# Optimization experiments

Hardware: AMD Instinct MI355X
Metric: run time of the kernel (lower is better)

Reference implementation:

```python
import jax, jax.numpy as jnp
from jax import lax
import numpy as np

V, D, H, E, L, B = 512, 128, 64, 4, 60, 4096
ADJ = 184  # ((180 + 7) // 8) * 8


def setup_inputs() -> dict:
    key = jax.random.key(0)
    it = iter(jax.random.split(key, 64))

    def nrm(shape, s=0.05):
        return jax.random.normal(next(it), shape, dtype=jnp.float32) * s

    x = jax.random.randint(next(it), (B, L), 0, V, dtype=jnp.int32)
    inp = {"x": x, "emb": nrm((V, D), 0.02).at[0].set(0.0)}  # padding_idx=0 row zero
    for d in ("f", "r"):
        inp[f"w_ih_{d}"] = nrm((4 * H, D)); inp[f"w_hh_{d}"] = nrm((4 * H, H))
        inp[f"b_ih_{d}"] = nrm((4 * H,)); inp[f"b_hh_{d}"] = nrm((4 * H,))
    for p, i_, h_, o_ in (("e", 1, 16, 8), ("l", 1, 16, 8), ("c", V, 32, 16), ("p", 6, 24, 12), ("x", 4, 16, 8)):
        inp[f"{p}_w1"] = nrm((h_, i_)); inp[f"{p}_b1"] = nrm((h_,))
        inp[f"{p}_w2"] = nrm((o_, h_)); inp[f"{p}_b2"] = nrm((o_,))
    inp["fp_w"] = nrm((ADJ, 180)); inp["fp_b"] = nrm((ADJ,))
    inp["attn_w"] = nrm((3 * ADJ, ADJ)); inp["attn_b"] = nrm((3 * ADJ,))
    inp["out_w"] = nrm((ADJ, ADJ)); inp["out_b"] = nrm((ADJ,))
    for i, (o_, i_) in enumerate(((128, ADJ), (64, 128), (32, 64), (E, 32)), 1):
        inp[f"g_w{i}"] = nrm((o_, i_)); inp[f"g_b{i}"] = nrm((o_,))
    return inp


def _mlp2(h, w1, b1, w2, b2):
    return jnp.maximum(h @ w1.T + b1, 0.0) @ w2.T + b2


def _lstm_final(xe, w_ih, w_hh, b_ih, b_hh):
    # torch LSTM gate order i, f, g, o; returns final hidden state [B, H]
    xg = jnp.einsum('bld,gd->blg', xe, w_ih) + b_ih
    h0 = jnp.zeros((xe.shape[0], H), xe.dtype)

    def step(carry, g_t):
        h, c = carry
        g = g_t + h @ w_hh.T + b_hh
        i, f, gg, o = jnp.split(g, 4, axis=-1)
        c = jax.nn.sigmoid(f) * c + jax.nn.sigmoid(i) * jnp.tanh(gg)
        h = jax.nn.sigmoid(o) * jnp.tanh(c)
        return (h, c), None

    (h, _), _ = lax.scan(step, (h0, h0), jnp.swapaxes(xg, 0, 1))
    return h


def _sequence_stats(x):
    # Fully vectorized equivalent of the per-sequence python loops
    f32 = jnp.float32
    mask = x != 0
    vlen = mask.sum(1)                                       # [B]
    vlenf = jnp.maximum(vlen, 1).astype(f32)
    pos = jnp.arange(L)
    # per-row histogram over valid tokens (torch.bincount of valid_seq)
    counts = jnp.zeros((B, V), f32).at[jnp.arange(B)[:, None], x].add(mask.astype(f32))
    probs = counts / jnp.maximum(counts.sum(1, keepdims=True), 1.0)
    entropy = -jnp.sum(probs * jnp.log(probs + 1e-8), axis=1)
    entropy = jnp.where(vlen > 1, entropy, 0.0)
    char_dist = counts / vlenf[:, None]
    # compact valid tokens to the front (torch: seq[seq != 0]), stable argsort
    order = jnp.argsort((~mask).astype(jnp.int32), axis=1)
    cseq = jnp.take_along_axis(x, order, axis=1)
    cseq = jnp.where(pos[None] < vlen[:, None], cseq, 0)
    a, b = cseq[:, :-1], cseq[:, 1:]
    pairmask = pos[: L - 1][None] < (vlen - 1)[:, None]
    den1 = jnp.maximum(vlen - 1, 1).astype(f32)
    repeat = ((a == b) & pairmask).sum(1) / den1
    inc = ((b > a) & pairmask).sum(1) / den1
    dec = ((b < a) & pairmask).sum(1) / den1
    m2 = pos[: L - 2][None] < (vlen - 2)[:, None]
    per = ((cseq[:, :-2] == cseq[:, 2:]) & m2).sum(1) / jnp.maximum(vlen - 2, 1)
    per = jnp.where(vlen >= 4, per, 0.0)
    diversity = (counts > 0).sum(1) / vlenf
    # longest run of equal consecutive tokens via cummax of reset positions
    eq = jnp.concatenate([jnp.zeros((B, 1), bool), (cseq[:, 1:] == cseq[:, :-1]) & (pos[1:][None] < vlen[:, None])], 1)
    lastreset = lax.cummax(jnp.where(eq, -1, pos[None]), axis=1)
    runlen = pos[None] - lastreset + 1
    max_rep = jnp.where(pos[None] < vlen[:, None], runlen, 0).max(1) / vlenf
    pattern = jnp.stack([repeat, inc, dec, per, diversity, max_rep], 1).astype(f32)
    pattern = jnp.where((vlen > 1)[:, None], pattern, 0.0)
    # unique bigrams: sort pair codes, count distinct valid codes
    codes = jnp.where(pairmask, a * V + b, -1)
    s = jnp.sort(codes, axis=1)
    prevc = jnp.concatenate([jnp.full((B, 1), -2, s.dtype), s[:, :-1]], 1)
    comp_ratio = ((s != prevc) & (s >= 0)).sum(1) / den1
    info_density = entropy / jnp.log(jnp.maximum(vlen, 2).astype(f32))
    # local complexity: mean over sliding windows of (#unique / w), w = min(5, len//2)
    wsel = jnp.minimum(5, vlen // 2)
    local = jnp.zeros((B,), f32)
    for w in (2, 3, 4, 5):
        nwin = L - w + 1
        sh = [cseq[:, k:k + nwin] for k in range(w)]
        u = jnp.ones((B, nwin), f32)
        for k in range(1, w):
            isnew = jnp.ones((B, nwin), bool)
            for m in range(k):
                isnew = isnew & (sh[k] != sh[m])
            u = u + isnew
        winmask = pos[:nwin][None] < (vlen - w + 1)[:, None]
        lc = (u * winmask).sum(1) / w / jnp.maximum(vlen - w + 1, 1)
        local = jnp.where(wsel == w, lc, local)
    trans = 1.0 - repeat  # transitions/(len-1) == 1 - repeat_ratio
    complexity = jnp.stack([comp_ratio, info_density, local, trans], 1).astype(f32)
    complexity = jnp.where((vlen > 1)[:, None], complexity, 0.0)
    return entropy, vlen, char_dist, pattern, complexity


def reference(x, emb, w_ih_f, w_hh_f, b_ih_f, b_hh_f, w_ih_r, w_hh_r, b_ih_r, b_hh_r, e_w1, e_b1, e_w2, e_b2, l_w1, l_b1, l_w2, l_b2, c_w1, c_b1, c_w2, c_b2, p_w1, p_b1, p_w2, p_b2, x_w1, x_b1, x_w2, x_b2, fp_w, fp_b, attn_w, attn_b, out_w, out_b, g_w1, g_b1, g_w2, g_b2, g_w3, g_b3, g_w4, g_b4):
    entropy, vlen, char_dist, pattern, complexity = _sequence_stats(x)
    xe = emb[x]                                               # [B, L, D]
    h_f = _lstm_final(xe, w_ih_f, w_hh_f, b_ih_f, b_hh_f)
    h_r = _lstm_final(xe[:, ::-1], w_ih_r, w_hh_r, b_ih_r, b_hh_r)
    feats = jnp.concatenate([
        h_f, h_r,
        _mlp2((entropy / 4.0)[:, None], e_w1, e_b1, e_w2, e_b2),
        _mlp2((vlen.astype(jnp.float32) / 60.0)[:, None], l_w1, l_b1, l_w2, l_b2),
        _mlp2(char_dist, c_w1, c_b1, c_w2, c_b2),
        _mlp2(pattern, p_w1, p_b1, p_w2, p_b2),
        _mlp2(complexity, x_w1, x_b1, x_w2, x_b2),
    ], axis=1)                                                # [B, 180]
    f = feats @ fp_w.T + fp_b                                 # [B, 184]
    # MultiheadAttention with seq_len == 1: softmax over a single key is 1,
    # so attended = out_proj(v_proj(f)) exactly (q/k projections cancel).
    wv, bv = attn_w[2 * ADJ:], attn_b[2 * ADJ:]
    attended = (f @ wv.T + bv) @ out_w.T + out_b
    h = jnp.maximum(attended @ g_w1.T + g_b1, 0.0)
    h = jnp.maximum(h @ g_w2.T + g_b2, 0.0)
    h = jnp.maximum(h @ g_w3.T + g_b3, 0.0)
    logits = h @ g_w4.T + g_b4
    return jax.nn.softmax(logits, axis=-1)  # eval path (training=False)
```

## Files before the change

### kernel.cpp

```cpp
#include <hip/hip_runtime.h>

#define BATCH 4096
#define SEQL  60
#define VOC   512
#define EMBD  128
#define HID   64
#define GATES 256
#define ADJ   184

typedef __attribute__((ext_vector_type(8))) short short8;
typedef __attribute__((ext_vector_type(4))) float f32x4;

__device__ __forceinline__ float sigm(float x) {
  return __builtin_amdgcn_rcpf(1.f + __expf(-x));
}
__device__ __forceinline__ float tanh_(float x) {
  float e = __expf(2.f * x);
  return 1.f - 2.f * __builtin_amdgcn_rcpf(e + 1.f);
}
__device__ __forceinline__ unsigned short f2bf_rne(float f) {
  unsigned int u = __float_as_uint(f);
  unsigned int r = (u + 0x7fffu + ((u >> 16) & 1u)) >> 16;
  return (unsigned short)r;
}
__device__ __forceinline__ unsigned short f2bf(float f) {
  return (unsigned short)((__float_as_uint(f) + 0x8000u) >> 16);
}
__device__ __forceinline__ float dot4(float4 a, float4 b, float acc) {
  acc = fmaf(a.x, b.x, acc); acc = fmaf(a.y, b.y, acc);
  acc = fmaf(a.z, b.z, acc); acc = fmaf(a.w, b.w, acc);
  return acc;
}
__device__ __forceinline__ float wsumf(float v) {
  #pragma unroll
  for (int s = 32; s > 0; s >>= 1) v += __shfl_xor(v, s, 64);
  return v;
}
__device__ __forceinline__ int wsumi(int v) {
  #pragma unroll
  for (int s = 32; s > 0; s >>= 1) v += __shfl_xor(v, s, 64);
  return v;
}
__device__ __forceinline__ int wmaxi(int v) {
  #pragma unroll
  for (int s = 32; s > 0; s >>= 1) v = max(v, __shfl_xor(v, s, 64));
  return v;
}

__global__ __launch_bounds__(256) void k_prep(
    const float* __restrict__ emb,
    const float* __restrict__ wih_f, const float* __restrict__ bif, const float* __restrict__ bhf,
    const float* __restrict__ wih_r, const float* __restrict__ bir, const float* __restrict__ bhr,
    const float* __restrict__ whh_f, const float* __restrict__ whh_r,
    const float* __restrict__ g_w1, const float* __restrict__ g_b1,
    const float* __restrict__ out_w, const float* __restrict__ out_b,
    const float* __restrict__ attn_w, const float* __restrict__ attn_b,
    const float* __restrict__ fp_w, const float* __restrict__ fp_b,
    const float* __restrict__ g_w2, const float* __restrict__ g_w3,
    const float* __restrict__ g_w4, const float* __restrict__ c_w1,
    float* __restrict__ G_f, float* __restrict__ G_r,
    unsigned short* __restrict__ Wfrag,
    float* __restrict__ A, float* __restrict__ avb,
    float* __restrict__ Bp, float* __restrict__ vb,
    float* __restrict__ g_w2t, float* __restrict__ g_w3t, float* __restrict__ g_w4t,
    float* __restrict__ c_w1t) {
  const int bid = blockIdx.x;
  const int tid = threadIdx.x;

  if (bid < 128) {
    const int dir = bid >> 6;
    const int rem = bid & 63;
    const int v0 = (rem >> 2) * 32;
    const int j0 = (rem & 3) * 64;
    const float* W = dir ? wih_r : wih_f;
    const float* bi = dir ? bir : bif;
    const float* bh = dir ? bhr : bhf;
    float* G = dir ? G_r : G_f;
    const int vp = tid >> 4;
    const int jq = tid & 15;
    const int v = v0 + vp * 2;
    const int j = j0 + jq * 4;
    const int gg = j >> 6;
    const int u0 = j & 63;

    const float4* E0 = (const float4*)(emb + (size_t)v * 128);
    const float4* E1 = (const float4*)(emb + (size_t)(v + 1) * 128);
    const float4* W0 = (const float4*)(W + (size_t)j * 128);
    const float4* W1 = (const float4*)(W + (size_t)(j + 1) * 128);
    const float4* W2 = (const float4*)(W + (size_t)(j + 2) * 128);
    const float4* W3 = (const float4*)(W + (size_t)(j + 3) * 128);

    float a00 = 0.f, a01 = 0.f, a02 = 0.f, a03 = 0.f;
    float a10 = 0.f, a11 = 0.f, a12 = 0.f, a13 = 0.f;
    #pragma unroll 4
    for (int d4 = 0; d4 < 32; d4++) {
      float4 e0 = E0[d4], e1 = E1[d4];
      float4 w0 = W0[d4], w1 = W1[d4], w2 = W2[d4], w3 = W3[d4];
      a00 = dot4(e0, w0, a00); a01 = dot4(e0, w1, a01);
      a02 = dot4(e0, w2, a02); a03 = dot4(e0, w3, a03);
      a10 = dot4(e1, w0, a10); a11 = dot4(e1, w1, a11);
      a12 = dot4(e1, w2, a12); a13 = dot4(e1, w3, a13);
    }
    float b0v = bi[j] + bh[j], b1v = bi[j + 1] + bh[j + 1];
    float b2v = bi[j + 2] + bh[j + 2], b3v = bi[j + 3] + bh[j + 3];
    float* g0 = G + (size_t)v * 256 + u0 * 4 + gg;
    g0[0]  = a00 + b0v; g0[4]  = a01 + b1v;
    g0[8]  = a02 + b2v; g0[12] = a03 + b3v;
    float* g1 = g0 + 256;
    g1[0]  = a10 + b0v; g1[4]  = a11 + b1v;
    g1[8]  = a12 + b2v; g1[12] = a13 + b3v;
  } else if (bid < 144) {
    const int id = (bid - 128) * 256 + tid;
    const int lane = id & 63;
    const int fc = id >> 6;
    const int c = fc & 1;
    const int gg = (fc >> 1) & 3;
    const int w = (fc >> 3) & 3;
    const int dir = fc >> 5;
    const float* whh = dir ? whh_r : whh_f;
    const int n = gg * 64 + w * 16 + (lane & 15);
    const int kb = c * 32 + (lane >> 4) * 8;
    unsigned short* o = Wfrag + (size_t)id * 8;
    #pragma unroll
    for (int j = 0; j < 8; j++) o[j] = f2bf_rne(whh[n * 64 + kb + j]);
  } else if (bid < 272) {
    const int i = bid - 144;
    const int j = tid;
    const float* g1r = g_w1 + (size_t)i * ADJ;
    if (j < ADJ) {
      float a0 = 0.f, a1 = 0.f, a2 = 0.f, a3 = 0.f;
      for (int k = 0; k < ADJ; k += 4) {
        a0 = fmaf(g1r[k],     out_w[(size_t)(k)     * ADJ + j], a0);
        a1 = fmaf(g1r[k + 1], out_w[(size_t)(k + 1) * ADJ + j], a1);
        a2 = fmaf(g1r[k + 2], out_w[(size_t)(k + 2) * ADJ + j], a2);
        a3 = fmaf(g1r[k + 3], out_w[(size_t)(k + 3) * ADJ + j], a3);
      }
      A[(size_t)i * ADJ + j] = (a0 + a1) + (a2 + a3);
    } else if (j == ADJ) {
      float a0 = 0.f;
      for (int k = 0; k < ADJ; k++) a0 = fmaf(g1r[k], out_b[k], a0);
      avb[i] = a0 + g_b1[i];
    }
  } else if (bid < 456) {
    const int k = bid - 272;
    const int j = tid;
    const float* wvr = attn_w + (size_t)(2 * ADJ + k) * ADJ;
    if (j < 180) {
      float a0 = 0.f, a1 = 0.f, a2 = 0.f, a3 = 0.f;
      for (int m = 0; m < ADJ; m += 4) {
        a0 = fmaf(wvr[m],     fp_w[(size_t)(m)     * 180 + j], a0);
        a1 = fmaf(wvr[m + 1], fp_w[(size_t)(m + 1) * 180 + j], a1);
        a2 = fmaf(wvr[m + 2], fp_w[(size_t)(m + 2) * 180 + j], a2);
        a3 = fmaf(wvr[m + 3], fp_w[(size_t)(m + 3) * 180 + j], a3);
      }
      Bp[(size_t)k * 180 + j] = (a0 + a1) + (a2 + a3);
    } else if (j == 180) {
      float a0 = 0.f;
      for (int m = 0; m < ADJ; m++) a0 = fmaf(wvr[m], fp_b[m], a0);
      vb[k] = a0 + attn_b[2 * ADJ + k];
    }
  } else if (bid == 456) {
    for (int i = tid; i < 64 * 128; i += 256) {
      int o = i >> 7, k = i & 127;
      g_w2t[k * 64 + o] = g_w2[i];
    }
    for (int i = tid; i < 32 * 64; i += 256) {
      int o = i >> 6, k = i & 63;
      g_w3t[k * 32 + o] = g_w3[i];
    }
    if (tid < 128) {
      int o = tid >> 5, k = tid & 31;
      g_w4t[k * 4 + o] = g_w4[tid];
    }
  } else {
    const int base = (bid - 457) * 2048;
    for (int i = tid; i < 2048; i += 256) {
      int idx = base + i;
      int o = idx >> 9, k = idx & 511;
      c_w1t[k * 32 + o] = k ? c_w1[o * 512 + k] : 0.f;
    }
  }
}

#define LSTM_STEP(T, CUR, NXT)                                                 \
  {                                                                            \
    const unsigned short* hb = hbuf[(T) & 1];                                  \
    short8 a0 = *(const short8*)(hb + ln * 72 + kg * 8);                       \
    short8 a1 = *(const short8*)(hb + ln * 72 + 32 + kg * 8);                  \
    if ((T) < 59) {                                                            \
      int tsn = dir ? (58 - (T)) : ((T) + 1);                                  \
      uint4 of4 = *(const uint4*)(tokoff + tsn * 16 + kg * 4);                 \
      NXT[0] = *(const float4*)(Gb + of4.x + ub);                              \
      NXT[1] = *(const float4*)(Gb + of4.y + ub);                              \
      NXT[2] = *(const float4*)(Gb + of4.z + ub);                              \
      NXT[3] = *(const float4*)(Gb + of4.w + ub);                              \
    }                                                                          \
    f32x4 z0 = {0.f, 0.f, 0.f, 0.f};                                           \
    f32x4 acc0 = z0, acc1 = z0, acc2 = z0, acc3 = z0;                          \
    acc0 = __builtin_amdgcn_mfma_f32_16x16x32_bf16(a0, bfr[0][0], acc0, 0, 0, 0); \
    acc1 = __builtin_amdgcn_mfma_f32_16x16x32_bf16(a0, bfr[1][0], acc1, 0, 0, 0); \
    acc2 = __builtin_amdgcn_mfma_f32_16x16x32_bf16(a0, bfr[2][0], acc2, 0, 0, 0); \
    acc3 = __builtin_amdgcn_mfma_f32_16x16x32_bf16(a0, bfr[3][0], acc3, 0, 0, 0); \
    acc0 = __builtin_amdgcn_mfma_f32_16x16x32_bf16(a1, bfr[0][1], acc0, 0, 0, 0); \
    acc1 = __builtin_amdgcn_mfma_f32_16x16x32_bf16(a1, bfr[1][1], acc1, 0, 0, 0); \
    acc2 = __builtin_amdgcn_mfma_f32_16x16x32_bf16(a1, bfr[2][1], acc2, 0, 0, 0); \
    acc3 = __builtin_amdgcn_mfma_f32_16x16x32_bf16(a1, bfr[3][1], acc3, 0, 0, 0); \
    unsigned short* hw = hbuf[((T) + 1) & 1];                                  \
    _Pragma("unroll")                                                          \
    for (int r = 0; r < 4; r++) {                                              \
      float gi = acc0[r] + CUR[r].x;                                           \
      float gf = acc1[r] + CUR[r].y;                                           \
      float gc = acc2[r] + CUR[r].z;                                           \
      float go = acc3[r] + CUR[r].w;                                           \
      float cn = sigm(gf) * cst[r] + sigm(gi) * tanh_(gc);                     \
      cst[r] = cn;                                                             \
      float h = sigm(go) * tanh_(cn);                                          \
      hw[(kg * 4 + r) * 72 + u] = f2bf(h);                                     \
      if ((T) == 59) ho[(size_t)(b0 + kg * 4 + r) * 64 + u] = h;               \
    }                                                                          \
    __syncthreads();                                                           \
  }

__global__ __launch_bounds__(256) void k_main(
    const int* __restrict__ x,
    const float* __restrict__ G_f, const float* __restrict__ G_r,
    const unsigned short* __restrict__ Wfrag,
    const float* __restrict__ A, const float* __restrict__ avb,
    const float* __restrict__ Bp, const float* __restrict__ vb,
    float* __restrict__ C1t, float* __restrict__ c1b,
    float* __restrict__ hf_o, float* __restrict__ hr_o,
    float* __restrict__ ent_o, float* __restrict__ vlen_o,
    float* __restrict__ pat_o, float* __restrict__ cpx_o) {
  __shared__ __align__(16) unsigned short hbuf[2][16 * 72];
  __shared__ __align__(16) unsigned int tokoff[60 * 16];
  __shared__ unsigned int cnt[4][512];
  __shared__ unsigned short q[4][68];
  const int bid = blockIdx.x;
  const int tid = threadIdx.x;

  if (bid < 512) {
    const int lane = tid & 63;
    const int w = tid >> 6;
    const int dir = bid >> 8;
    const int blk = bid & 255;
    const int b0 = blk << 4;
    const float* G = dir ? G_r : G_f;
    const char* Gb = (const char*)G;
    float* ho = dir ? hr_o : hf_o;

    for (int i = tid; i < 960; i += 256) {
      int r = i / 60, t = i - r * 60;
      tokoff[t * 16 + r] = ((unsigned int)x[(size_t)(b0 + r) * 60 + t]) << 10;
    }
    for (int i = tid; i < 16 * 72; i += 256) hbuf[0][i] = 0;

    short8 bfr[4][2];
    #pragma unroll
    for (int gg = 0; gg < 4; gg++)
      #pragma unroll
      for (int c = 0; c < 2; c++) {
        int idx = (((dir * 4 + w) * 4 + gg) * 2 + c) * 64 + lane;
        bfr[gg][c] = *(const short8*)(Wfrag + (size_t)idx * 8);
      }

    const int kg = lane >> 4;
    const int ln = lane & 15;
    const int u = w * 16 + ln;
    const unsigned int ub = (unsigned int)u * 16;
    float cst[4] = {0.f, 0.f, 0.f, 0.f};
    float4 gvA[4], gvB[4];

    __syncthreads();

    {
      int ts0 = dir ? 59 : 0;
      uint4 of4 = *(const uint4*)(tokoff + ts0 * 16 + kg * 4);
      gvA[0] = *(const float4*)(Gb + of4.x + ub);
      gvA[1] = *(const float4*)(Gb + of4.y + ub);
      gvA[2] = *(const float4*)(Gb + of4.z + ub);
      gvA[3] = *(const float4*)(Gb + of4.w + ub);
    }

    #pragma unroll 1
    for (int tt = 0; tt < 30; tt++) {
      const int t0 = tt * 2, t1 = tt * 2 + 1;
      LSTM_STEP(t0, gvA, gvB)
      LSTM_STEP(t1, gvB, gvA)
    }
  } else if (bid < 1536) {
    const int lane = tid & 63;
    const int wid = tid >> 6;
    const int row = (bid - 512) * 4 + wid;
    unsigned int* cr = cnt[wid];
    unsigned short* qr = q[wid];

    for (int i = lane; i < 512; i += 64) cr[i] = 0u;
    qr[lane] = 0;
    if (lane < 4) qr[64 + lane] = 0;
    int v = (lane < 60) ? x[row * 60 + lane] : 0;
    bool act = (v != 0);
    unsigned long long amask = __ballot(act);
    int n = __popcll(amask);
    __syncthreads();
    if (act) {
      int pos = __popcll(amask & ((1ull << lane) - 1ull));
      qr[pos] = (unsigned short)v;
      atomicAdd(&cr[v], 1u);
    }
    __syncthreads();

    float vlenf = (float)(n >= 1 ? n : 1);
    float inv = 1.f / vlenf;

    float ent = 0.f; int distinct = 0;
    #pragma unroll
    for (int j = 0; j < 8; j++) {
      unsigned int c = cr[lane + j * 64];
      if (c) {
        distinct++;
        float p = (float)c * inv;
        ent -= p * __logf(p + 1e-8f);
      }
    }
    ent = wsumf(ent);
    distinct = wsumi(distinct);

    int a = qr[lane], b = qr[lane + 1], c2 = qr[lane + 2];
    bool v1 = (lane + 1 < n);
    bool v2 = (lane + 2 < n);
    int rep  = __popcll(__ballot(v1 && (a == b)));
    int incs = __popcll(__ballot(v1 && (b > a)));
    int decs = __popcll(__ballot(v1 && (b < a)));
    int per2 = __popcll(__ballot(v2 && (a == c2)));

    int prev = (lane > 0) ? (int)qr[lane - 1] : -1;
    bool isst = (lane < n) && (lane == 0 || a != prev);
    unsigned long long smask = __ballot(isst);
    int len = 0;
    if (isst) {
      unsigned long long hi = (lane < 63) ? (smask >> (lane + 1)) : 0ull;
      int next = hi ? (lane + __ffsll((unsigned long long)hi)) : n;
      len = next - lane;
    }
    int maxrun = wmaxi(len);

    int code = v1 ? (a * VOC + b) : -1;
    int unique = v1 ? 1 : 0;
    #pragma unroll 1
    for (int j = 0; j < 58; j++) {
      int cj = __shfl(code, j, 64);
      if (j < lane && cj == code) unique = 0;
    }
    int dc = __popcll(__ballot(unique != 0));

    int wl = n >> 1; if (wl > 5) wl = 5;
    float local = 0.f;
    if (wl >= 2) {
      bool pv = (lane + wl <= n);
      int u = 0;
      if (pv) {
        int t0 = qr[lane], t1 = qr[lane + 1], t2 = qr[lane + 2];
        int t3 = qr[lane + 3], t4 = qr[lane + 4];
        u = 1;
        u += (t1 != t0);
        if (wl >= 3) u += (int)((t2 != t1) && (t2 != t0));
        if (wl >= 4) u += (int)((t3 != t2) && (t3 != t1) && (t3 != t0));
        if (wl >= 5) u += (int)((t4 != t3) && (t4 != t2) && (t4 != t1) && (t4 != t0));
      }
      int usum = wsumi(u);
      int denw = n - wl + 1; if (denw < 1) denw = 1;
      local = (float)usum / (float)wl / (float)denw;
    }

    float den1 = (float)((n - 1) >= 1 ? (n - 1) : 1);
    float repeat = (float)rep / den1;
    float per = (n >= 4) ? (float)per2 / (float)((n - 2) >= 1 ? (n - 2) : 1) : 0.f;
    float entz = (n > 1) ? ent : 0.f;
    float z = (n > 1) ? 1.f : 0.f;

    if (lane == 0) {
      ent_o[row] = entz;
      vlen_o[row] = (float)n;
      pat_o[row * 6 + 0] = repeat * z;
      pat_o[row * 6 + 1] = (float)incs / den1 * z;
      pat_o[row * 6 + 2] = (float)decs / den1 * z;
      pat_o[row * 6 + 3] = per * z;
      pat_o[row * 6 + 4] = (float)distinct * inv * z;
      pat_o[row * 6 + 5] = (float)maxrun * inv * z;
      cpx_o[row * 4 + 0] = (float)dc / den1 * z;
      cpx_o[row * 4 + 1] = entz / __logf((float)(n >= 2 ? n : 2)) * z;
      cpx_o[row * 4 + 2] = local * z;
      cpx_o[row * 4 + 3] = (1.f - repeat) * z;
    }
  } else {
    const int i = bid - 1536, j = tid;
    const float* Ar = A + (size_t)i * ADJ;
    if (j < 180) {
      float a0 = 0.f, a1 = 0.f, a2 = 0.f, a3 = 0.f;
      for (int k = 0; k < ADJ; k += 4) {
        a0 = fmaf(Ar[k],     Bp[(size_t)(k)     * 180 + j], a0);
        a1 = fmaf(Ar[k + 1], Bp[(size_t)(k + 1) * 180 + j], a1);
        a2 = fmaf(Ar[k + 2], Bp[(size_t)(k + 2) * 180 + j], a2);
        a3 = fmaf(Ar[k + 3], Bp[(size_t)(k + 3) * 180 + j], a3);
      }
      C1t[(size_t)j * 128 + i] = (a0 + a1) + (a2 + a3);
    } else if (j == 180) {
      float a0 = 0.f;
      for (int k = 0; k < ADJ; k++) a0 = fmaf(Ar[k], vb[k], a0);
      c1b[i] = a0 + avb[i];
    }
  }
}

#define FSTR 192

__global__ __launch_bounds__(256) void k_head(
    const int* __restrict__ x,
    const float* __restrict__ hf, const float* __restrict__ hr,
    const float* __restrict__ ent, const float* __restrict__ vlen,
    const float* __restrict__ pat, const float* __restrict__ cpx,
    const float* __restrict__ e_w1, const float* __restrict__ e_b1,
    const float* __restrict__ e_w2, const float* __restrict__ e_b2,
    const float* __restrict__ l_w1, const float* __restrict__ l_b1,
    const float* __restrict__ l_w2, const float* __restrict__ l_b2,
    const float* __restrict__ c_w1t, const float* __restrict__ c_b1,
    const float* __restrict__ c_w2, const float* __restrict__ c_b2,
    const float* __restrict__ p_w1, const float* __restrict__ p_b1,
    const float* __restrict__ p_w2, const float* __restrict__ p_b2,
    const float* __restrict__ x_w1, const float* __restrict__ x_b1,
    const float* __restrict__ x_w2, const float* __restrict__ x_b2,
    const float* __restrict__ C1t, const float* __restrict__ c1b,
    const float* __restrict__ g_w2t, const float* __restrict__ g_b2,
    const float* __restrict__ g_w3t, const float* __restrict__ g_b3,
    const float* __restrict__ g_w4t, const float* __restrict__ g_b4,
    float* __restrict__ out) {
  __shared__ float feat[8 * FSTR];
  __shared__ unsigned short tk[8 * 64];
  __shared__ float h1[8 * 128];
  __shared__ float h2[8 * 64];
  __shared__ float h3[8 * 32];
  __shared__ float h1c[8 * 33];
  __shared__ float lg[32];
  const int tid = threadIdx.x;
  const int b0 = blockIdx.x * 8;

  if (tid < 128) {
    int r = tid >> 4, c = tid & 15;
    float4 vv = ((const float4*)(hf + (size_t)(b0 + r) * 64))[c];
    *(float4*)(feat + r * FSTR + c * 4) = vv;
  } else {
    int t = tid - 128;
    int r = t >> 4, c = t & 15;
    float4 vv = ((const float4*)(hr + (size_t)(b0 + r) * 64))[c];
    *(float4*)(feat + r * FSTR + 64 + c * 4) = vv;
  }
  for (int i = tid; i < 480; i += 256) {
    int r = i / 60, t = i - r * 60;
    tk[r * 64 + t] = (unsigned short)x[(size_t)(b0 + r) * 60 + t];
  }
  __syncthreads();
  {
    int o = tid & 31, r = tid >> 5;
    const unsigned short* tkr = tk + r * 64;
    float a0 = 0.f, a1 = 0.f, a2 = 0.f, a3 = 0.f;
    #pragma unroll 5
    for (int t = 0; t < 60; t += 4) {
      int t0 = tkr[t], t1 = tkr[t + 1], t2 = tkr[t + 2], t3 = tkr[t + 3];
      a0 += c_w1t[t0 * 32 + o];
      a1 += c_w1t[t1 * 32 + o];
      a2 += c_w1t[t2 * 32 + o];
      a3 += c_w1t[t3 * 32 + o];
    }
    float invv = __builtin_amdgcn_rcpf(fmaxf(vlen[b0 + r], 1.f));
    h1c[r * 33 + o] = fmaxf(((a0 + a1) + (a2 + a3)) * invv + c_b1[o], 0.f);
  }
  __syncthreads();
  if (tid < 32) {
    const int m = tid & 3, r = tid >> 2, b = b0 + r;
    float tt[24];
    if (m == 0) {
      float ein = ent[b] * 0.25f;
      #pragma unroll
      for (int o = 0; o < 16; o++) tt[o] = fmaxf(e_w1[o] * ein + e_b1[o], 0.f);
      #pragma unroll
      for (int o = 0; o < 8; o++) {
        float a = e_b2[o];
        #pragma unroll
        for (int k = 0; k < 16; k++) a = fmaf(e_w2[o * 16 + k], tt[k], a);
        feat[r * FSTR + 128 + o] = a;
      }
    } else if (m == 1) {
      float lin = vlen[b] * (1.f / 60.f);
      #pragma unroll
      for (int o = 0; o < 16; o++) tt[o] = fmaxf(l_w1[o] * lin + l_b1[o], 0.f);
      #pragma unroll
      for (int o = 0; o < 8; o++) {
        float a = l_b2[o];
        #pragma unroll
        for (int k = 0; k < 16; k++) a = fmaf(l_w2[o * 16 + k], tt[k], a);
        feat[r * FSTR + 136 + o] = a;
      }
    } else if (m == 2) {
      float pin[6];
      #pragma unroll
      for (int k = 0; k < 6; k++) pin[k] = pat[b * 6 + k];
      #pragma unroll
      for (int o = 0; o < 24; o++) {
        float a = p_b1[o];
        #pragma unroll
        for (int k = 0; k < 6; k++) a = fmaf(p_w1[o * 6 + k], pin[k], a);
        tt[o] = fmaxf(a, 0.f);
      }
      #pragma unroll
      for (int o = 0; o < 12; o++) {
        float a = p_b2[o];
        #pragma unroll
        for (int k = 0; k < 24; k++) a = fmaf(p_w2[o * 24 + k], tt[k], a);
        feat[r * FSTR + 160 + o] = a;
      }
    } else {
      float xin[4];
      #pragma unroll
      for (int k = 0; k < 4; k++) xin[k] = cpx[b * 4 + k];
      #pragma unroll
      for (int o = 0; o < 16; o++) {
        float a = x_b1[o];
        #pragma unroll
        for (int k = 0; k < 4; k++) a = fmaf(x_w1[o * 4 + k], xin[k], a);
        tt[o] = fmaxf(a, 0.f);
      }
      #pragma unroll
      for (int o = 0; o < 8; o++) {
        float a = x_b2[o];
        #pragma unroll
        for (int k = 0; k < 16; k++) a = fmaf(x_w2[o * 16 + k], tt[k], a);
        feat[r * FSTR + 172 + o] = a;
      }
    }
  } else if (tid >= 64 && tid < 192) {
    int t = tid - 64;
    int r = t >> 4, o = t & 15;
    float a = c_b2[o];
    const float* hh = h1c + r * 33;
    #pragma unroll
    for (int k = 0; k < 32; k++) a = fmaf(c_w2[o * 32 + k], hh[k], a);
    feat[r * FSTR + 144 + o] = a;
  }
  __syncthreads();

  {
    const int o = tid & 127, rg = tid >> 7;
    const float* f0p = feat + (rg * 4 + 0) * FSTR;
    const float* f1p = feat + (rg * 4 + 1) * FSTR;
    const float* f2p = feat + (rg * 4 + 2) * FSTR;
    const float* f3p = feat + (rg * 4 + 3) * FSTR;
    float a0 = 0.f, a1 = 0.f, a2 = 0.f, a3 = 0.f;
    #pragma unroll 3
    for (int k4 = 0; k4 < 45; k4++) {
      float w0 = C1t[(size_t)(k4 * 4 + 0) * 128 + o];
      float w1 = C1t[(size_t)(k4 * 4 + 1) * 128 + o];
      float w2 = C1t[(size_t)(k4 * 4 + 2) * 128 + o];
      float w3 = C1t[(size_t)(k4 * 4 + 3) * 128 + o];
      float4 f0 = *(const float4*)(f0p + k4 * 4);
      float4 f1 = *(const float4*)(f1p + k4 * 4);
      float4 f2 = *(const float4*)(f2p + k4 * 4);
      float4 f3 = *(const float4*)(f3p + k4 * 4);
      a0 = fmaf(w0, f0.x, a0); a0 = fmaf(w1, f0.y, a0);
      a0 = fmaf(w2, f0.z, a0); a0 = fmaf(w3, f0.w, a0);
      a1 = fmaf(w0, f1.x, a1); a1 = fmaf(w1, f1.y, a1);
      a1 = fmaf(w2, f1.z, a1); a1 = fmaf(w3, f1.w, a1);
      a2 = fmaf(w0, f2.x, a2); a2 = fmaf(w1, f2.y, a2);
      a2 = fmaf(w2, f2.z, a2); a2 = fmaf(w3, f2.w, a2);
      a3 = fmaf(w0, f3.x, a3); a3 = fmaf(w1, f3.y, a3);
      a3 = fmaf(w2, f3.z, a3); a3 = fmaf(w3, f3.w, a3);
    }
    float bb = c1b[o];
    h1[(rg * 4 + 0) * 128 + o] = fmaxf(a0 + bb, 0.f);
    h1[(rg * 4 + 1) * 128 + o] = fmaxf(a1 + bb, 0.f);
    h1[(rg * 4 + 2) * 128 + o] = fmaxf(a2 + bb, 0.f);
    h1[(rg * 4 + 3) * 128 + o] = fmaxf(a3 + bb, 0.f);
  }
  __syncthreads();
  {
    const int o = tid & 63, rg = tid >> 6;
    const float* f0p = h1 + (rg * 2 + 0) * 128;
    const float* f1p = h1 + (rg * 2 + 1) * 128;
    float a0 = 0.f, a1 = 0.f;
    #pragma unroll 4
    for (int k4 = 0; k4 < 32; k4++) {
      float w0 = g_w2t[(k4 * 4 + 0) * 64 + o];
      float w1 = g_w2t[(k4 * 4 + 1) * 64 + o];
      float w2 = g_w2t[(k4 * 4 + 2) * 64 + o];
      float w3 = g_w2t[(k4 * 4 + 3) * 64 + o];
      float4 f0 = *(const float4*)(f0p + k4 * 4);
      float4 f1 = *(const float4*)(f1p + k4 * 4);
      a0 = fmaf(w0, f0.x, a0); a0 = fmaf(w1, f0.y, a0);
      a0 = fmaf(w2, f0.z, a0); a0 = fmaf(w3, f0.w, a0);
      a1 = fmaf(w0, f1.x, a1); a1 = fmaf(w1, f1.y, a1);
      a1 = fmaf(w2, f1.z, a1); a1 = fmaf(w3, f1.w, a1);
    }
    float bb = g_b2[o];
    h2[(rg * 2 + 0) * 64 + o] = fmaxf(a0 + bb, 0.f);
    h2[(rg * 2 + 1) * 64 + o] = fmaxf(a1 + bb, 0.f);
  }
  __syncthreads();
  {
    const int o = tid & 31, rg = tid >> 5;
    const float* fp = h2 + rg * 64;
    float a = 0.f;
    #pragma unroll 4
    for (int k4 = 0; k4 < 16; k4++) {
      float w0 = g_w3t[(k4 * 4 + 0) * 32 + o];
      float w1 = g_w3t[(k4 * 4 + 1) * 32 + o];
      float w2 = g_w3t[(k4 * 4 + 2) * 32 + o];
      float w3 = g_w3t[(k4 * 4 + 3) * 32 + o];
      float4 f0 = *(const float4*)(fp + k4 * 4);
      a = fmaf(w0, f0.x, a); a = fmaf(w1, f0.y, a);
      a = fmaf(w2, f0.z, a); a = fmaf(w3, f0.w, a);
    }
    h3[rg * 32 + o] = fmaxf(a + g_b3[o], 0.f);
  }
  __syncthreads();
  if (tid < 32) {
    int r = tid >> 2, o = tid & 3;
    const float* hh = h3 + r * 32;
    float a = g_b4[o];
    #pragma unroll
    for (int k = 0; k < 32; k++) a = fmaf(g_w4t[k * 4 + o], hh[k], a);
    lg[tid] = a;
  }
  __syncthreads();
  if (tid < 8) {
    float l0 = lg[tid * 4 + 0], l1 = lg[tid * 4 + 1];
    float l2 = lg[tid * 4 + 2], l3 = lg[tid * 4 + 3];
    float m = fmaxf(fmaxf(l0, l1), fmaxf(l2, l3));
    float e0 = __expf(l0 - m), e1 = __expf(l1 - m);
    float e2 = __expf(l2 - m), e3 = __expf(l3 - m);
    float is = __builtin_amdgcn_rcpf(e0 + e1 + e2 + e3);
    float4 o4; o4.x = e0 * is; o4.y = e1 * is; o4.z = e2 * is; o4.w = e3 * is;
    *(float4*)(out + (size_t)(b0 + tid) * 4) = o4;
  }
}

extern "C" void kernel_launch(void* const* d_in, const int* in_sizes, int n_in,
                              void* d_out, int out_size, void* d_ws, size_t ws_size,
                              hipStream_t stream) {
  const int*   x     = (const int*)d_in[0];
  const float* emb   = (const float*)d_in[1];
  const float* wih_f = (const float*)d_in[2];
  const float* whh_f = (const float*)d_in[3];
  const float* bih_f = (const float*)d_in[4];
  const float* bhh_f = (const float*)d_in[5];
  const float* wih_r = (const float*)d_in[6];
  const float* whh_r = (const float*)d_in[7];
  const float* bih_r = (const float*)d_in[8];
  const float* bhh_r = (const float*)d_in[9];
  const float* e_w1 = (const float*)d_in[10]; const float* e_b1 = (const float*)d_in[11];
  const float* e_w2 = (const float*)d_in[12]; const float* e_b2 = (const float*)d_in[13];
  const float* l_w1 = (const float*)d_in[14]; const float* l_b1 = (const float*)d_in[15];
  const float* l_w2 = (const float*)d_in[16]; const float* l_b2 = (const float*)d_in[17];
  const float* c_w1 = (const float*)d_in[18]; const float* c_b1 = (const float*)d_in[19];
  const float* c_w2 = (const float*)d_in[20]; const float* c_b2 = (const float*)d_in[21];
  const float* p_w1 = (const float*)d_in[22]; const float* p_b1 = (const float*)d_in[23];
  const float* p_w2 = (const float*)d_in[24]; const float* p_b2 = (const float*)d_in[25];
  const float* x_w1 = (const float*)d_in[26]; const float* x_b1 = (const float*)d_in[27];
  const float* x_w2 = (const float*)d_in[28]; const float* x_b2 = (const float*)d_in[29];
  const float* fp_w = (const float*)d_in[30]; const float* fp_b = (const float*)d_in[31];
  const float* attn_w = (const float*)d_in[32]; const float* attn_b = (const float*)d_in[33];
  const float* out_w = (const float*)d_in[34]; const float* out_b = (const float*)d_in[35];
  const float* g_w1 = (const float*)d_in[36]; const float* g_b1 = (const float*)d_in[37];
  const float* g_w2 = (const float*)d_in[38]; const float* g_b2 = (const float*)d_in[39];
  const float* g_w3 = (const float*)d_in[40]; const float* g_b3 = (const float*)d_in[41];
  const float* g_w4 = (const float*)d_in[42]; const float* g_b4 = (const float*)d_in[43];

  float* ws   = (float*)d_ws;
  float* G_f  = ws;
  float* G_r  = G_f  + 512 * 256;
  float* hfw  = G_r  + 512 * 256;
  float* hrw  = hfw  + BATCH * 64;
  float* entw = hrw  + BATCH * 64;
  float* vlnw = entw + BATCH;
  float* patw = vlnw + BATCH;
  float* cpxw = patw + BATCH * 6;
  float* Aw   = cpxw + BATCH * 4;
  float* avbw = Aw + 128 * ADJ;
  float* Bpw  = avbw + 128;
  float* vbw  = Bpw + ADJ * 180;
  float* C1t  = vbw + ADJ;
  float* c1b  = C1t + 180 * 128;
  float* g2t  = c1b + 128;
  float* g3t  = g2t + 128 * 64;
  float* g4t  = g3t + 64 * 32;
  float* cw1t = g4t + 32 * 4;
  unsigned short* Wfrag = (unsigned short*)(cw1t + 512 * 32);

  k_prep<<<dim3(465), dim3(256), 0, stream>>>(
      emb, wih_f, bih_f, bhh_f, wih_r, bih_r, bhh_r, whh_f, whh_r,
      g_w1, g_b1, out_w, out_b, attn_w, attn_b, fp_w, fp_b,
      g_w2, g_w3, g_w4, c_w1,
      G_f, G_r, Wfrag, Aw, avbw, Bpw, vbw, g2t, g3t, g4t, cw1t);
  k_main<<<dim3(1664), dim3(256), 0, stream>>>(
      x, G_f, G_r, Wfrag, Aw, avbw, Bpw, vbw, C1t, c1b,
      hfw, hrw, entw, vlnw, patw, cpxw);
  k_head<<<dim3(BATCH / 8), dim3(256), 0, stream>>>(
      x, hfw, hrw, entw, vlnw, patw, cpxw,
      e_w1, e_b1, e_w2, e_b2, l_w1, l_b1, l_w2, l_b2,
      cw1t, c_b1, c_w2, c_b2, p_w1, p_b1, p_w2, p_b2,
      x_w1, x_b1, x_w2, x_b2, C1t, c1b,
      g2t, g_b2, g3t, g_b3, g4t, g_b4,
      (float*)d_out);
}
```

Measured before the change: 247.3 us.

## Fuse head kernel into main kernel using global flag-based dependencies

Merges the separate head kernel into the main kernel as extra blocks. The head blocks wait on per-block global flags set by the LSTM, stats and prep2 blocks, with a counter for the C1 matrix build. Shared memory becomes a single overlaid byte buffer, and arguments move into one struct. The intent is to remove a launch boundary and let head work overlap the tail of the LSTM. This relies on spin-waiting blocks making forward progress, which risks deadlock or stalls if waiting blocks occupy slots needed by the producer blocks. It also adds a memset launch.

```diff
diff --git a/kernel.cpp b/kernel.cpp
--- a/kernel.cpp
+++ b/kernel.cpp
@@ -3,9 +3,6 @@
 #define BATCH 4096
 #define SEQL  60
 #define VOC   512
-#define EMBD  128
-#define HID   64
-#define GATES 256
 #define ADJ   184
 
 typedef __attribute__((ext_vector_type(8))) short short8;
@@ -20,8 +17,7 @@
 }
 __device__ __forceinline__ unsigned short f2bf_rne(float f) {
   unsigned int u = __float_as_uint(f);
-  unsigned int r = (u + 0x7fffu + ((u >> 16) & 1u)) >> 16;
-  return (unsigned short)r;
+  return (unsigned short)((u + 0x7fffu + ((u >> 16) & 1u)) >> 16);
 }
 __device__ __forceinline__ unsigned short f2bf(float f) {
   return (unsigned short)((__float_as_uint(f) + 0x8000u) >> 16);
@@ -47,23 +43,37 @@
   return v;
 }
 
-__global__ __launch_bounds__(256) void k_prep(
-    const float* __restrict__ emb,
-    const float* __restrict__ wih_f, const float* __restrict__ bif, const float* __restrict__ bhf,
-    const float* __restrict__ wih_r, const float* __restrict__ bir, const float* __restrict__ bhr,
-    const float* __restrict__ whh_f, const float* __restrict__ whh_r,
-    const float* __restrict__ g_w1, const float* __restrict__ g_b1,
-    const float* __restrict__ out_w, const float* __restrict__ out_b,
-    const float* __restrict__ attn_w, const float* __restrict__ attn_b,
-    const float* __restrict__ fp_w, const float* __restrict__ fp_b,
-    const float* __restrict__ g_w2, const float* __restrict__ g_w3,
-    const float* __restrict__ g_w4, const float* __restrict__ c_w1,
-    float* __restrict__ G_f, float* __restrict__ G_r,
-    unsigned short* __restrict__ Wfrag,
-    float* __restrict__ A, float* __restrict__ avb,
-    float* __restrict__ Bp, float* __restrict__ vb,
-    float* __restrict__ g_w2t, float* __restrict__ g_w3t, float* __restrict__ g_w4t,
-    float* __restrict__ c_w1t) {
+struct KP {
+  const int* x;
+  const float *emb, *wih_f, *bif, *bhf, *wih_r, *bir, *bhr, *whh_f, *whh_r;
+  const float *e_w1, *e_b1, *e_w2, *e_b2, *l_w1, *l_b1, *l_w2, *l_b2;
+  const float *c_w1, *c_b1, *c_w2, *c_b2, *p_w1, *p_b1, *p_w2, *p_b2;
+  const float *x_w1, *x_b1, *x_w2, *x_b2;
+  const float *fp_w, *fp_b, *attn_w, *attn_b, *out_w, *out_b;
+  const float *g_w1, *g_b1, *g_w2, *g_b2, *g_w3, *g_b3, *g_w4, *g_b4;
+  float *G_f, *G_r;
+  unsigned short* Wfrag;
+  float *A, *avb, *Bp, *vb, *C1t, *c1b, *g2t, *g3t, *g4t, *cw1t;
+  float *hf, *hr, *ent, *vlen, *pat, *cpx;
+  int *lflag, *sflag, *p2ctr;
+  float* out;
+};
+
+#define SM_BYTES 15616
+#define SM_HBUF  0
+#define SM_TOK   4608
+#define SM_CNT   0
+#define SM_Q     8192
+#define SM_FEAT  0
+#define SM_TK    6144
+#define SM_H1    7168
+#define SM_H2    11264
+#define SM_H3    13312
+#define SM_H1C   14336
+#define SM_LG    15392
+#define FSTR 192
+
+__global__ __launch_bounds__(256) void k_prep(KP p) {
   const int bid = blockIdx.x;
   const int tid = threadIdx.x;
 
@@ -72,19 +82,17 @@
     const int rem = bid & 63;
     const int v0 = (rem >> 2) * 32;
     const int j0 = (rem & 3) * 64;
-    const float* W = dir ? wih_r : wih_f;
-    const float* bi = dir ? bir : bif;
-    const float* bh = dir ? bhr : bhf;
-    float* G = dir ? G_r : G_f;
-    const int vp = tid >> 4;
-    const int jq = tid & 15;
-    const int v = v0 + vp * 2;
-    const int j = j0 + jq * 4;
+    const float* W = dir ? p.wih_r : p.wih_f;
+    const float* bi = dir ? p.bir : p.bif;
+    const float* bh = dir ? p.bhr : p.bhf;
+    float* G = dir ? p.G_r : p.G_f;
+    const int v = v0 + (tid >> 4) * 2;
+    const int j = j0 + (tid & 15) * 4;
     const int gg = j >> 6;
     const int u0 = j & 63;
 
-    const float4* E0 = (const float4*)(emb + (size_t)v * 128);
-    const float4* E1 = (const float4*)(emb + (size_t)(v + 1) * 128);
+    const float4* E0 = (const float4*)(p.emb + (size_t)v * 128);
+    const float4* E1 = (const float4*)(p.emb + (size_t)(v + 1) * 128);
     const float4* W0 = (const float4*)(W + (size_t)j * 128);
     const float4* W1 = (const float4*)(W + (size_t)(j + 1) * 128);
     const float4* W2 = (const float4*)(W + (size_t)(j + 2) * 128);
@@ -117,74 +125,74 @@
     const int gg = (fc >> 1) & 3;
     const int w = (fc >> 3) & 3;
     const int dir = fc >> 5;
-    const float* whh = dir ? whh_r : whh_f;
+    const float* whh = dir ? p.whh_r : p.whh_f;
     const int n = gg * 64 + w * 16 + (lane & 15);
     const int kb = c * 32 + (lane >> 4) * 8;
-    unsigned short* o = Wfrag + (size_t)id * 8;
+    unsigned short* o = p.Wfrag + (size_t)id * 8;
     #pragma unroll
     for (int j = 0; j < 8; j++) o[j] = f2bf_rne(whh[n * 64 + kb + j]);
   } else if (bid < 272) {
     const int i = bid - 144;
     const int j = tid;
-    const float* g1r = g_w1 + (size_t)i * ADJ;
+    const float* g1r = p.g_w1 + (size_t)i * ADJ;
     if (j < ADJ) {
       float a0 = 0.f, a1 = 0.f, a2 = 0.f, a3 = 0.f;
       for (int k = 0; k < ADJ; k += 4) {
-        a0 = fmaf(g1r[k],     out_w[(size_t)(k)     * ADJ + j], a0);
-        a1 = fmaf(g1r[k + 1], out_w[(size_t)(k + 1) * ADJ + j], a1);
-        a2 = fmaf(g1r[k + 2], out_w[(size_t)(k + 2) * ADJ + j], a2);
-        a3 = fmaf(g1r[k + 3], out_w[(size_t)(k + 3) * ADJ + j], a3);
+        a0 = fmaf(g1r[k],     p.out_w[(size_t)(k)     * ADJ + j], a0);
+        a1 = fmaf(g1r[k + 1], p.out_w[(size_t)(k + 1) * ADJ + j], a1);
+        a2 = fmaf(g1r[k + 2], p.out_w[(size_t)(k + 2) * ADJ + j], a2);
+        a3 = fmaf(g1r[k + 3], p.out_w[(size_t)(k + 3) * ADJ + j], a3);
       }
-      A[(size_t)i * ADJ + j] = (a0 + a1) + (a2 + a3);
+      p.A[(size_t)i * ADJ + j] = (a0 + a1) + (a2 + a3);
     } else if (j == ADJ) {
       float a0 = 0.f;
-      for (int k = 0; k < ADJ; k++) a0 = fmaf(g1r[k], out_b[k], a0);
-      avb[i] = a0 + g_b1[i];
+      for (int k = 0; k < ADJ; k++) a0 = fmaf(g1r[k], p.out_b[k], a0);
+      p.avb[i] = a0 + p.g_b1[i];
     }
   } else if (bid < 456) {
     const int k = bid - 272;
     const int j = tid;
-    const float* wvr = attn_w + (size_t)(2 * ADJ + k) * ADJ;
+    const float* wvr = p.attn_w + (size_t)(2 * ADJ + k) * ADJ;
     if (j < 180) {
       float a0 = 0.f, a1 = 0.f, a2 = 0.f, a3 = 0.f;
       for (int m = 0; m < ADJ; m += 4) {
-        a0 = fmaf(wvr[m],     fp_w[(size_t)(m)     * 180 + j], a0);
-        a1 = fmaf(wvr[m + 1], fp_w[(size_t)(m + 1) * 180 + j], a1);
-        a2 = fmaf(wvr[m + 2], fp_w[(size_t)(m + 2) * 180 + j], a2);
-        a3 = fmaf(wvr[m + 3], fp_w[(size_t)(m + 3) * 180 + j], a3);
+        a0 = fmaf(wvr[m],     p.fp_w[(size_t)(m)     * 180 + j], a0);
+        a1 = fmaf(wvr[m + 1], p.fp_w[(size_t)(m + 1) * 180 + j], a1);
+        a2 = fmaf(wvr[m + 2], p.fp_w[(size_t)(m + 2) * 180 + j], a2);
+        a3 = fmaf(wvr[m + 3], p.fp_w[(size_t)(m + 3) * 180 + j], a3);
       }
-      Bp[(size_t)k * 180 + j] = (a0 + a1) + (a2 + a3);
+      p.Bp[(size_t)k * 180 + j] = (a0 + a1) + (a2 + a3);
     } else if (j == 180) {
       float a0 = 0.f;
-      for (int m = 0; m < ADJ; m++) a0 = fmaf(wvr[m], fp_b[m], a0);
-      vb[k] = a0 + attn_b[2 * ADJ + k];
+      for (int m = 0; m < ADJ; m++) a0 = fmaf(wvr[m], p.fp_b[m], a0);
+      p.vb[k] = a0 + p.attn_b[2 * ADJ + k];
     }
   } else if (bid == 456) {
     for (int i = tid; i < 64 * 128; i += 256) {
       int o = i >> 7, k = i & 127;
-      g_w2t[k * 64 + o] = g_w2[i];
+      p.g2t[k * 64 + o] = p.g_w2[i];
     }
     for (int i = tid; i < 32 * 64; i += 256) {
       int o = i >> 6, k = i & 63;
-      g_w3t[k * 32 + o] = g_w3[i];
+      p.g3t[k * 32 + o] = p.g_w3[i];
     }
     if (tid < 128) {
       int o = tid >> 5, k = tid & 31;
-      g_w4t[k * 4 + o] = g_w4[tid];
+      p.g4t[k * 4 + o] = p.g_w4[tid];
     }
   } else {
     const int base = (bid - 457) * 2048;
     for (int i = tid; i < 2048; i += 256) {
       int idx = base + i;
       int o = idx >> 9, k = idx & 511;
-      c_w1t[k * 32 + o] = k ? c_w1[o * 512 + k] : 0.f;
+      p.cw1t[k * 32 + o] = k ? p.c_w1[o * 512 + k] : 0.f;
     }
   }
 }
 
 #define LSTM_STEP(T, CUR, NXT)                                                 \
   {                                                                            \
-    const unsigned short* hb = hbuf[(T) & 1];                                  \
+    const unsigned short* hb = hbuf + ((T) & 1) * (16 * 72);                   \
     short8 a0 = *(const short8*)(hb + ln * 72 + kg * 8);                       \
     short8 a1 = *(const short8*)(hb + ln * 72 + 32 + kg * 8);                  \
     if ((T) < 59) {                                                            \
@@ -205,7 +213,7 @@
     acc1 = __builtin_amdgcn_mfma_f32_16x16x32_bf16(a1, bfr[1][1], acc1, 0, 0, 0); \
     acc2 = __builtin_amdgcn_mfma_f32_16x16x32_bf16(a1, bfr[2][1], acc2, 0, 0, 0); \
     acc3 = __builtin_amdgcn_mfma_f32_16x16x32_bf16(a1, bfr[3][1], acc3, 0, 0, 0); \
-    unsigned short* hw = hbuf[((T) + 1) & 1];                                  \
+    unsigned short* hw = hbuf + (((T) + 1) & 1) * (16 * 72);                   \
     _Pragma("unroll")                                                          \
     for (int r = 0; r < 4; r++) {                                              \
       float gi = acc0[r] + CUR[r].x;                                           \
@@ -221,242 +229,228 @@
     __syncthreads();                                                           \
   }
 
-__global__ __launch_bounds__(256) void k_main(
-    const int* __restrict__ x,
-    const float* __restrict__ G_f, const float* __restrict__ G_r,
-    const unsigned short* __restrict__ Wfrag,
-    const float* __restrict__ A, const float* __restrict__ avb,
-    const float* __restrict__ Bp, const float* __restrict__ vb,
-    float* __restrict__ C1t, float* __restrict__ c1b,
-    float* __restrict__ hf_o, float* __restrict__ hr_o,
-    float* __restrict__ ent_o, float* __restrict__ vlen_o,
-    float* __restrict__ pat_o, float* __restrict__ cpx_o) {
-  __shared__ __align__(16) unsigned short hbuf[2][16 * 72];
-  __shared__ __align__(16) unsigned int tokoff[60 * 16];
-  __shared__ unsigned int cnt[4][512];
-  __shared__ unsigned short q[4][68];
-  const int bid = blockIdx.x;
-  const int tid = threadIdx.x;
-
-  if (bid < 512) {
-    const int lane = tid & 63;
-    const int w = tid >> 6;
-    const int dir = bid >> 8;
-    const int blk = bid & 255;
-    const int b0 = blk << 4;
-    const float* G = dir ? G_r : G_f;
-    const char* Gb = (const char*)G;
-    float* ho = dir ? hr_o : hf_o;
-
-    for (int i = tid; i < 960; i += 256) {
-      int r = i / 60, t = i - r * 60;
-      tokoff[t * 16 + r] = ((unsigned int)x[(size_t)(b0 + r) * 60 + t]) << 10;
-    }
-    for (int i = tid; i < 16 * 72; i += 256) hbuf[0][i] = 0;
-
-    short8 bfr[4][2];
+__device__ void lstm_block(int bid, int tid, const KP& p, char* smem) {
+  unsigned short* hbuf = (unsigned short*)(smem + SM_HBUF);
+  unsigned int* tokoff = (unsigned int*)(smem + SM_TOK);
+  const int lane = tid & 63;
+  const int w = tid >> 6;
+  const int dir = bid >> 8;
+  const int blk = bid & 255;
+  const int b0 = blk << 4;
+  const float* G = dir ? p.G_r : p.G_f;
+  const char* Gb = (const char*)G;
+  float* ho = dir ? p.hr : p.hf;
+
+  for (int i = tid; i < 960; i += 256) {
+    int r = i / 60, t = i - r * 60;
+    tokoff[t * 16 + r] = ((unsigned int)p.x[(size_t)(b0 + r) * 60 + t]) << 10;
+  }
+  for (int i = tid; i < 16 * 72; i += 256) hbuf[i] = 0;
+
+  short8 bfr[4][2];
+  #pragma unroll
+  for (int gg = 0; gg < 4; gg++)
     #pragma unroll
-    for (int gg = 0; gg < 4; gg++)
-      #pragma unroll
-      for (int c = 0; c < 2; c++) {
-        int idx = (((dir * 4 + w) * 4 + gg) * 2 + c) * 64 + lane;
-        bfr[gg][c] = *(const short8*)(Wfrag + (size_t)idx * 8);
-      }
-
-    const int kg = lane >> 4;
-    const int ln = lane & 15;
-    const int u = w * 16 + ln;
-    const unsigned int ub = (unsigned int)u * 16;
-    float cst[4] = {0.f, 0.f, 0.f, 0.f};
-    float4 gvA[4], gvB[4];
-
-    __syncthreads();
-
-    {
-      int ts0 = dir ? 59 : 0;
-      uint4 of4 = *(const uint4*)(tokoff + ts0 * 16 + kg * 4);
-      gvA[0] = *(const float4*)(Gb + of4.x + ub);
-      gvA[1] = *(const float4*)(Gb + of4.y + ub);
-      gvA[2] = *(const float4*)(Gb + of4.z + ub);
-      gvA[3] = *(const float4*)(Gb + of4.w + ub);
-    }
-
-    #pragma unroll 1
-    for (int tt = 0; tt < 30; tt++) {
-      const int t0 = tt * 2, t1 = tt * 2 + 1;
-      LSTM_STEP(t0, gvA, gvB)
-      LSTM_STEP(t1, gvB, gvA)
-    }
-  } else if (bid < 1536) {
-    const int lane = tid & 63;
-    const int wid = tid >> 6;
-    const int row = (bid - 512) * 4 + wid;
-    unsigned int* cr = cnt[wid];
-    unsigned short* qr = q[wid];
-
-    for (int i = lane; i < 512; i += 64) cr[i] = 0u;
-    qr[lane] = 0;
-    if (lane < 4) qr[64 + lane] = 0;
-    int v = (lane < 60) ? x[row * 60 + lane] : 0;
-    bool act = (v != 0);
-    unsigned long long amask = __ballot(act);
-    int n = __popcll(amask);
-    __syncthreads();
-    if (act) {
-      int pos = __popcll(amask & ((1ull << lane) - 1ull));
-      qr[pos] = (unsigned short)v;
-      atomicAdd(&cr[v], 1u);
-    }
-    __syncthreads();
-
-    float vlenf = (float)(n >= 1 ? n : 1);
-    float inv = 1.f / vlenf;
-
-    float ent = 0.f; int distinct = 0;
-    #pragma unroll
-    for (int j = 0; j < 8; j++) {
-      unsigned int c = cr[lane + j * 64];
-      if (c) {
-        distinct++;
-        float p = (float)c * inv;
-        ent -= p * __logf(p + 1e-8f);
-      }
-    }
-    ent = wsumf(ent);
-    distinct = wsumi(distinct);
-
-    int a = qr[lane], b = qr[lane + 1], c2 = qr[lane + 2];
-    bool v1 = (lane + 1 < n);
-    bool v2 = (lane + 2 < n);
-    int rep  = __popcll(__ballot(v1 && (a == b)));
-    int incs = __popcll(__ballot(v1 && (b > a)));
-    int decs = __popcll(__ballot(v1 && (b < a)));
-    int per2 = __popcll(__ballot(v2 && (a == c2)));
-
-    int prev = (lane > 0) ? (int)qr[lane - 1] : -1;
-    bool isst = (lane < n) && (lane == 0 || a != prev);
-    unsigned long long smask = __ballot(isst);
-    int len = 0;
-    if (isst) {
-      unsigned long long hi = (lane < 63) ? (smask >> (lane + 1)) : 0ull;
-      int next = hi ? (lane + __ffsll((unsigned long long)hi)) : n;
-      len = next - lane;
-    }
-    int maxrun = wmaxi(len);
-
-    int code = v1 ? (a * VOC + b) : -1;
-    int unique = v1 ? 1 : 0;
-    #pragma unroll 1
-    for (int j = 0; j < 58; j++) {
-      int cj = __shfl(code, j, 64);
-      if (j < lane && cj == code) unique = 0;
-    }
-    int dc = __popcll(__ballot(unique != 0));
-
-    int wl = n >> 1; if (wl > 5) wl = 5;
-    float local = 0.f;
-    if (wl >= 2) {
-      bool pv = (lane + wl <= n);
-      int u = 0;
-      if (pv) {
-        int t0 = qr[lane], t1 = qr[lane + 1], t2 = qr[lane + 2];
-        int t3 = qr[lane + 3], t4 = qr[lane + 4];
-        u = 1;
-        u += (t1 != t0);
-        if (wl >= 3) u += (int)((t2 != t1) && (t2 != t0));
-        if (wl >= 4) u += (int)((t3 != t2) && (t3 != t1) && (t3 != t0));
-        if (wl >= 5) u += (int)((t4 != t3) && (t4 != t2) && (t4 != t1) && (t4 != t0));
-      }
-      int usum = wsumi(u);
-      int denw = n - wl + 1; if (denw < 1) denw = 1;
-      local = (float)usum / (float)wl / (float)denw;
-    }
-
-    float den1 = (float)((n - 1) >= 1 ? (n - 1) : 1);
-    float repeat = (float)rep / den1;
-    float per = (n >= 4) ? (float)per2 / (float)((n - 2) >= 1 ? (n - 2) : 1) : 0.f;
-    float entz = (n > 1) ? ent : 0.f;
-    float z = (n > 1) ? 1.f : 0.f;
-
-    if (lane == 0) {
-      ent_o[row] = entz;
-      vlen_o[row] = (float)n;
-      pat_o[row * 6 + 0] = repeat * z;
-      pat_o[row * 6 + 1] = (float)incs / den1 * z;
-      pat_o[row * 6 + 2] = (float)decs / den1 * z;
-      pat_o[row * 6 + 3] = per * z;
-      pat_o[row * 6 + 4] = (float)distinct * inv * z;
-      pat_o[row * 6 + 5] = (float)maxrun * inv * z;
-      cpx_o[row * 4 + 0] = (float)dc / den1 * z;
-      cpx_o[row * 4 + 1] = entz / __logf((float)(n >= 2 ? n : 2)) * z;
-      cpx_o[row * 4 + 2] = local * z;
-      cpx_o[row * 4 + 3] = (1.f - repeat) * z;
-    }
-  } else {
-    const int i = bid - 1536, j = tid;
-    const float* Ar = A + (size_t)i * ADJ;
-    if (j < 180) {
-      float a0 = 0.f, a1 = 0.f, a2 = 0.f, a3 = 0.f;
-      for (int k = 0; k < ADJ; k += 4) {
-        a0 = fmaf(Ar[k],     Bp[(size_t)(k)     * 180 + j], a0);
-        a1 = fmaf(Ar[k + 1], Bp[(size_t)(k + 1) * 180 + j], a1);
-        a2 = fmaf(Ar[k + 2], Bp[(size_t)(k + 2) * 180 + j], a2);
-        a3 = fmaf(Ar[k + 3], Bp[(size_t)(k + 3) * 180 + j], a3);
-      }
-      C1t[(size_t)j * 128 + i] = (a0 + a1) + (a2 + a3);
-    } else if (j == 180) {
-      float a0 = 0.f;
-      for (int k = 0; k < ADJ; k++) a0 = fmaf(Ar[k], vb[k], a0);
-      c1b[i] = a0 + avb[i];
-    }
-  }
-}
-
-#define FSTR 192
-
-__global__ __launch_bounds__(256) void k_head(
-    const int* __restrict__ x,
-    const float* __restrict__ hf, const float* __restrict__ hr,
-    const float* __restrict__ ent, const float* __restrict__ vlen,
-    const float* __restrict__ pat, const float* __restrict__ cpx,
-    const float* __restrict__ e_w1, const float* __restrict__ e_b1,
-    const float* __restrict__ e_w2, const float* __restrict__ e_b2,
-    const float* __restrict__ l_w1, const float* __restrict__ l_b1,
-    const float* __restrict__ l_w2, const float* __restrict__ l_b2,
-    const float* __restrict__ c_w1t, const float* __restrict__ c_b1,
-    const float* __restrict__ c_w2, const float* __restrict__ c_b2,
-    const float* __restrict__ p_w1, const float* __restrict__ p_b1,
-    const float* __restrict__ p_w2, const float* __restrict__ p_b2,
-    const float* __restrict__ x_w1, const float* __restrict__ x_b1,
-    const float* __restrict__ x_w2, const float* __restrict__ x_b2,
-    const float* __restrict__ C1t, const float* __restrict__ c1b,
-    const float* __restrict__ g_w2t, const float* __restrict__ g_b2,
-    const float* __restrict__ g_w3t, const float* __restrict__ g_b3,
-    const float* __restrict__ g_w4t, const float* __restrict__ g_b4,
-    float* __restrict__ out) {
-  __shared__ float feat[8 * FSTR];
-  __shared__ unsigned short tk[8 * 64];
-  __shared__ float h1[8 * 128];
-  __shared__ float h2[8 * 64];
-  __shared__ float h3[8 * 32];
-  __shared__ float h1c[8 * 33];
-  __shared__ float lg[32];
-  const int tid = threadIdx.x;
-  const int b0 = blockIdx.x * 8;
+    for (int c = 0; c < 2; c++) {
+      int idx = (((dir * 4 + w) * 4 + gg) * 2 + c) * 64 + lane;
+      bfr[gg][c] = *(const short8*)(p.Wfrag + (size_t)idx * 8);
+    }
+
+  const int kg = lane >> 4;
+  const int ln = lane & 15;
+  const int u = w * 16 + ln;
+  const unsigned int ub = (unsigned int)u * 16;
+  float cst[4] = {0.f, 0.f, 0.f, 0.f};
+  float4 gvA[4], gvB[4];
+
+  __syncthreads();
+
+  {
+    int ts0 = dir ? 59 : 0;
+    uint4 of4 = *(const uint4*)(tokoff + ts0 * 16 + kg * 4);
+    gvA[0] = *(const float4*)(Gb + of4.x + ub);
+    gvA[1] = *(const float4*)(Gb + of4.y + ub);
+    gvA[2] = *(const float4*)(Gb + of4.z + ub);
+    gvA[3] = *(const float4*)(Gb + of4.w + ub);
+  }
+
+  #pragma unroll 1
+  for (int tt = 0; tt < 30; tt++) {
+    const int t0 = tt * 2, t1 = tt * 2 + 1;
+    LSTM_STEP(t0, gvA, gvB)
+    LSTM_STEP(t1, gvB, gvA)
+  }
+  __threadfence();
+  __syncthreads();
+  if (tid == 0) atomicExch(&p.lflag[bid], 1);
+}
+
+__device__ void prep2_block(int i, int j, const KP& p) {
+  const float* Ar = p.A + (size_t)i * ADJ;
+  if (j < 180) {
+    float a0 = 0.f, a1 = 0.f, a2 = 0.f, a3 = 0.f;
+    for (int k = 0; k < ADJ; k += 4) {
+      a0 = fmaf(Ar[k],     p.Bp[(size_t)(k)     * 180 + j], a0);
+      a1 = fmaf(Ar[k + 1], p.Bp[(size_t)(k + 1) * 180 + j], a1);
+      a2 = fmaf(Ar[k + 2], p.Bp[(size_t)(k + 2) * 180 + j], a2);
+      a3 = fmaf(Ar[k + 3], p.Bp[(size_t)(k + 3) * 180 + j], a3);
+    }
+    p.C1t[(size_t)j * 128 + i] = (a0 + a1) + (a2 + a3);
+  } else if (j == 180) {
+    float a0 = 0.f;
+    for (int k = 0; k < ADJ; k++) a0 = fmaf(Ar[k], p.vb[k], a0);
+    p.c1b[i] = a0 + p.avb[i];
+  }
+  __threadfence();
+  __syncthreads();
+  if (j == 0) atomicAdd(p.p2ctr, 1);
+}
+
+__device__ void stats_block(int s, int tid, const KP& p, char* smem) {
+  unsigned int* cntb = (unsigned int*)(smem + SM_CNT);
+  unsigned short* qb = (unsigned short*)(smem + SM_Q);
+  const int lane = tid & 63;
+  const int wid = tid >> 6;
+  const int row = s * 4 + wid;
+  unsigned int* cr = cntb + wid * 512;
+  unsigned short* qr = qb + wid * 68;
+
+  for (int i = lane; i < 512; i += 64) cr[i] = 0u;
+  qr[lane] = 0;
+  if (lane < 4) qr[64 + lane] = 0;
+  int v = (lane < 60) ? p.x[row * 60 + lane] : 0;
+  bool act = (v != 0);
+  unsigned long long amask = __ballot(act);
+  int n = __popcll(amask);
+  __syncthreads();
+  if (act) {
+    int pos = __popcll(amask & ((1ull << lane) - 1ull));
+    qr[pos] = (unsigned short)v;
+    atomicAdd(&cr[v], 1u);
+  }
+  __syncthreads();
+
+  float vlenf = (float)(n >= 1 ? n : 1);
+  float inv = 1.f / vlenf;
+
+  float ent = 0.f; int distinct = 0;
+  #pragma unroll
+  for (int j = 0; j < 8; j++) {
+    unsigned int c = cr[lane + j * 64];
+    if (c) {
+      distinct++;
+      float pr = (float)c * inv;
+      ent -= pr * __logf(pr + 1e-8f);
+    }
+  }
+  ent = wsumf(ent);
+  distinct = wsumi(distinct);
+
+  int a = qr[lane], b = qr[lane + 1], c2 = qr[lane + 2];
+  bool v1 = (lane + 1 < n);
+  bool v2 = (lane + 2 < n);
+  int rep  = __popcll(__ballot(v1 && (a == b)));
+  int incs = __popcll(__ballot(v1 && (b > a)));
+  int decs = __popcll(__ballot(v1 && (b < a)));
+  int per2 = __popcll(__ballot(v2 && (a == c2)));
+
+  int prev = (lane > 0) ? (int)qr[lane - 1] : -1;
+  bool isst = (lane < n) && (lane == 0 || a != prev);
+  unsigned long long smask = __ballot(isst);
+  int len = 0;
+  if (isst) {
+    unsigned long long hi = (lane < 63) ? (smask >> (lane + 1)) : 0ull;
+    int next = hi ? (lane + __ffsll((unsigned long long)hi)) : n;
+    len = next - lane;
+  }
+  int maxrun = wmaxi(len);
+
+  int code = v1 ? (a * VOC + b) : -1;
+  int unique = v1 ? 1 : 0;
+  #pragma unroll 1
+  for (int j = 0; j < 58; j++) {
+    int cj = __shfl(code, j, 64);
+    if (j < lane && cj == code) unique = 0;
+  }
+  int dc = __popcll(__ballot(unique != 0));
+
+  int wl = n >> 1; if (wl > 5) wl = 5;
+  float local = 0.f;
+  if (wl >= 2) {
+    bool pv = (lane + wl <= n);
+    int u = 0;
+    if (pv) {
+      int t0 = qr[lane], t1 = qr[lane + 1], t2 = qr[lane + 2];
+      int t3 = qr[lane + 3], t4 = qr[lane + 4];
+      u = 1;
+      u += (t1 != t0);
+      if (wl >= 3) u += (int)((t2 != t1) && (t2 != t0));
+      if (wl >= 4) u += (int)((t3 != t2) && (t3 != t1) && (t3 != t0));
+      if (wl >= 5) u += (int)((t4 != t3) && (t4 != t2) && (t4 != t1) && (t4 != t0));
+    }
+    int usum = wsumi(u);
+    int denw = n - wl + 1; if (denw < 1) denw = 1;
+    local = (float)usum / (float)wl / (float)denw;
+  }
+
+  float den1 = (float)((n - 1) >= 1 ? (n - 1) : 1);
+  float repeat = (float)rep / den1;
+  float per = (n >= 4) ? (float)per2 / (float)((n - 2) >= 1 ? (n - 2) : 1) : 0.f;
+  float entz = (n > 1) ? ent : 0.f;
+  float z = (n > 1) ? 1.f : 0.f;
+
+  if (lane == 0) {
+    p.ent[row] = entz;
+    p.vlen[row] = (float)n;
+    p.pat[row * 6 + 0] = repeat * z;
+    p.pat[row * 6 + 1] = (float)incs / den1 * z;
+    p.pat[row * 6 + 2] = (float)decs / den1 * z;
+    p.pat[row * 6 + 3] = per * z;
+    p.pat[row * 6 + 4] = (float)distinct * inv * z;
+    p.pat[row * 6 + 5] = (float)maxrun * inv * z;
+    p.cpx[row * 4 + 0] = (float)dc / den1 * z;
+    p.cpx[row * 4 + 1] = entz / __logf((float)(n >= 2 ? n : 2)) * z;
+    p.cpx[row * 4 + 2] = local * z;
+    p.cpx[row * 4 + 3] = (1.f - repeat) * z;
+  }
+  __threadfence();
+  __syncthreads();
+  if (tid == 0) atomicExch(&p.sflag[s], 1);
+}
+
+__device__ void head_block(int hb, int tid, const KP& p, char* smem) {
+  if (tid == 0) {
+    while (atomicAdd(p.p2ctr, 0) < 128) __builtin_amdgcn_s_sleep(16);
+    while (atomicAdd(&p.lflag[hb >> 1], 0) == 0) __builtin_amdgcn_s_sleep(16);
+    while (atomicAdd(&p.lflag[256 + (hb >> 1)], 0) == 0) __builtin_amdgcn_s_sleep(16);
+    while (atomicAdd(&p.sflag[hb * 2], 0) == 0) __builtin_amdgcn_s_sleep(16);
+    while (atomicAdd(&p.sflag[hb * 2 + 1], 0) == 0) __builtin_amdgcn_s_sleep(16);
+    __threadfence();
+  }
+  __syncthreads();
+
+  float* feat = (float*)(smem + SM_FEAT);
+  unsigned short* tk = (unsigned short*)(smem + SM_TK);
+  float* h1 = (float*)(smem + SM_H1);
+  float* h2 = (float*)(smem + SM_H2);
+  float* h3 = (float*)(smem + SM_H3);
+  float* h1c = (float*)(smem + SM_H1C);
+  float* lg = (float*)(smem + SM_LG);
+  const int b0 = hb * 8;
 
   if (tid < 128) {
     int r = tid >> 4, c = tid & 15;
-    float4 vv = ((const float4*)(hf + (size_t)(b0 + r) * 64))[c];
+    float4 vv = ((const float4*)(p.hf + (size_t)(b0 + r) * 64))[c];
     *(float4*)(feat + r * FSTR + c * 4) = vv;
   } else {
     int t = tid - 128;
     int r = t >> 4, c = t & 15;
-    float4 vv = ((const float4*)(hr + (size_t)(b0 + r) * 64))[c];
+    float4 vv = ((const float4*)(p.hr + (size_t)(b0 + r) * 64))[c];
     *(float4*)(feat + r * FSTR + 64 + c * 4) = vv;
   }
   for (int i = tid; i < 480; i += 256) {
     int r = i / 60, t = i - r * 60;
-    tk[r * 64 + t] = (unsigned short)x[(size_t)(b0 + r) * 60 + t];
+    tk[r * 64 + t] = (unsigned short)p.x[(size_t)(b0 + r) * 60 + t];
   }
   __syncthreads();
   {
@@ -466,84 +460,84 @@
     #pragma unroll 5
     for (int t = 0; t < 60; t += 4) {
       int t0 = tkr[t], t1 = tkr[t + 1], t2 = tkr[t + 2], t3 = tkr[t + 3];
-      a0 += c_w1t[t0 * 32 + o];
-      a1 += c_w1t[t1 * 32 + o];
-      a2 += c_w1t[t2 * 32 + o];
-      a3 += c_w1t[t3 * 32 + o];
-    }
-    float invv = __builtin_amdgcn_rcpf(fmaxf(vlen[b0 + r], 1.f));
-    h1c[r * 33 + o] = fmaxf(((a0 + a1) + (a2 + a3)) * invv + c_b1[o], 0.f);
+      a0 += p.cw1t[t0 * 32 + o];
+      a1 += p.cw1t[t1 * 32 + o];
+      a2 += p.cw1t[t2 * 32 + o];
+      a3 += p.cw1t[t3 * 32 + o];
+    }
+    float invv = __builtin_amdgcn_rcpf(fmaxf(p.vlen[b0 + r], 1.f));
+    h1c[r * 33 + o] = fmaxf(((a0 + a1) + (a2 + a3)) * invv + p.c_b1[o], 0.f);
   }
   __syncthreads();
   if (tid < 32) {
     const int m = tid & 3, r = tid >> 2, b = b0 + r;
     float tt[24];
     if (m == 0) {
-      float ein = ent[b] * 0.25f;
-      #pragma unroll
-      for (int o = 0; o < 16; o++) tt[o] = fmaxf(e_w1[o] * ein + e_b1[o], 0.f);
+      float ein = p.ent[b] * 0.25f;
+      #pragma unroll
+      for (int o = 0; o < 16; o++) tt[o] = fmaxf(p.e_w1[o] * ein + p.e_b1[o], 0.f);
       #pragma unroll
       for (int o = 0; o < 8; o++) {
-        float a = e_b2[o];
+        float a = p.e_b2[o];
         #pragma unroll
-        for (int k = 0; k < 16; k++) a = fmaf(e_w2[o * 16 + k], tt[k], a);
+        for (int k = 0; k < 16; k++) a = fmaf(p.e_w2[o * 16 + k], tt[k], a);
         feat[r * FSTR + 128 + o] = a;
       }
     } else if (m == 1) {
-      float lin = vlen[b] * (1.f / 60.f);
-      #pragma unroll
-      for (int o = 0; o < 16; o++) tt[o] = fmaxf(l_w1[o] * lin + l_b1[o], 0.f);
+      float lin = p.vlen[b] * (1.f / 60.f);
+      #pragma unroll
+      for (int o = 0; o < 16; o++) tt[o] = fmaxf(p.l_w1[o] * lin + p.l_b1[o], 0.f);
       #pragma unroll
       for (int o = 0; o < 8; o++) {
-        float a = l_b2[o];
+        float a = p.l_b2[o];
         #pragma unroll
-        for (int k = 0; k < 16; k++) a = fmaf(l_w2[o * 16 + k], tt[k], a);
+        for (int k = 0; k < 16; k++) a = fmaf(p.l_w2[o * 16 + k], tt[k], a);
         feat[r * FSTR + 136 + o] = a;
       }
     } else if (m == 2) {
       float pin[6];
       #pragma unroll
-      for (int k = 0; k < 6; k++) pin[k] = pat[b * 6 + k];
+      for (int k = 0; k < 6; k++) pin[k] = p.pat[b * 6 + k];
       #pragma unroll
       for (int o = 0; o < 24; o++) {
-        float a = p_b1[o];
+        float a = p.p_b1[o];
         #pragma unroll
-        for (int k = 0; k < 6; k++) a = fmaf(p_w1[o * 6 + k], pin[k], a);
+        for (int k = 0; k < 6; k++) a = fmaf(p.p_w1[o * 6 + k], pin[k], a);
         tt[o] = fmaxf(a, 0.f);
       }
       #pragma unroll
       for (int o = 0; o < 12; o++) {
-        float a = p_b2[o];
+        float a = p.p_b2[o];
         #pragma unroll
-        for (int k = 0; k < 24; k++) a = fmaf(p_w2[o * 24 + k], tt[k], a);
+        for (int k = 0; k < 24; k++) a = fmaf(p.p_w2[o * 24 + k], tt[k], a);
         feat[r * FSTR + 160 + o] = a;
       }
     } else {
       float xin[4];
       #pragma unroll
-      for (int k = 0; k < 4; k++) xin[k] = cpx[b * 4 + k];
+      for (int k = 0; k < 4; k++) xin[k] = p.cpx[b * 4 + k];
       #pragma unroll
       for (int o = 0; o < 16; o++) {
-        float a = x_b1[o];
+        float a = p.x_b1[o];
         #pragma unroll
-        for (int k = 0; k < 4; k++) a = fmaf(x_w1[o * 4 + k], xin[k], a);
+        for (int k = 0; k < 4; k++) a = fmaf(p.x_w1[o * 4 + k], xin[k], a);
         tt[o] = fmaxf(a, 0.f);
       }
       #pragma unroll
       for (int o = 0; o < 8; o++) {
-        float a = x_b2[o];
+        float a = p.x_b2[o];
         #pragma unroll
-        for (int k = 0; k < 16; k++) a = fmaf(x_w2[o * 16 + k], tt[k], a);
+        for (int k = 0; k < 16; k++) a = fmaf(p.x_w2[o * 16 + k], tt[k], a);
         feat[r * FSTR + 172 + o] = a;
       }
     }
   } else if (tid >= 64 && tid < 192) {
     int t = tid - 64;
     int r = t >> 4, o = t & 15;
-    float a = c_b2[o];
+    float a = p.c_b2[o];
     const float* hh = h1c + r * 33;
     #pragma unroll
-    for (int k = 0; k < 32; k++) a = fmaf(c_w2[o * 32 + k], hh[k], a);
+    for (int k = 0; k < 32; k++) a = fmaf(p.c_w2[o * 32 + k], hh[k], a);
     feat[r * FSTR + 144 + o] = a;
   }
   __syncthreads();
@@ -557,10 +551,10 @@
     float a0 = 0.f, a1 = 0.f, a2 = 0.f, a3 = 0.f;
     #pragma unroll 3
     for (int k4 = 0; k4 < 45; k4++) {
-      float w0 = C1t[(size_t)(k4 * 4 + 0) * 128 + o];
-      float w1 = C1t[(size_t)(k4 * 4 + 1) * 128 + o];
-      float w2 = C1t[(size_t)(k4 * 4 + 2) * 128 + o];
-      float w3 = C1t[(size_t)(k4 * 4 + 3) * 128 + o];
+      float w0 = p.C1t[(size_t)(k4 * 4 + 0) * 128 + o];
+      float w1 = p.C1t[(size_t)(k4 * 4 + 1) * 128 + o];
+      float w2 = p.C1t[(size_t)(k4 * 4 + 2) * 128 + o];
+      float w3 = p.C1t[(size_t)(k4 * 4 + 3) * 128 + o];
       float4 f0 = *(const float4*)(f0p + k4 * 4);
       float4 f1 = *(const float4*)(f1p + k4 * 4);
       float4 f2 = *(const float4*)(f2p + k4 * 4);
@@ -574,7 +568,7 @@
       a3 = fmaf(w0, f3.x, a3); a3 = fmaf(w1, f3.y, a3);
       a3 = fmaf(w2, f3.z, a3); a3 = fmaf(w3, f3.w, a3);
     }
-    float bb = c1b[o];
+    float bb = p.c1b[o];
     h1[(rg * 4 + 0) * 128 + o] = fmaxf(a0 + bb, 0.f);
     h1[(rg * 4 + 1) * 128 + o] = fmaxf(a1 + bb, 0.f);
     h1[(rg * 4 + 2) * 128 + o] = fmaxf(a2 + bb, 0.f);
@@ -588,10 +582,10 @@
     float a0 = 0.f, a1 = 0.f;
     #pragma unroll 4
     for (int k4 = 0; k4 < 32; k4++) {
-      float w0 = g_w2t[(k4 * 4 + 0) * 64 + o];
-      float w1 = g_w2t[(k4 * 4 + 1) * 64 + o];
-      float w2 = g_w2t[(k4 * 4 + 2) * 64 + o];
-      float w3 = g_w2t[(k4 * 4 + 3) * 64 + o];
+      float w0 = p.g2t[(k4 * 4 + 0) * 64 + o];
+      float w1 = p.g2t[(k4 * 4 + 1) * 64 + o];
+      float w2 = p.g2t[(k4 * 4 + 2) * 64 + o];
+      float w3 = p.g2t[(k4 * 4 + 3) * 64 + o];
       float4 f0 = *(const float4*)(f0p + k4 * 4);
       float4 f1 = *(const float4*)(f1p + k4 * 4);
       a0 = fmaf(w0, f0.x, a0); a0 = fmaf(w1, f0.y, a0);
@@ -599,7 +593,7 @@
       a1 = fmaf(w0, f1.x, a1); a1 = fmaf(w1, f1.y, a1);
       a1 = fmaf(w2, f1.z, a1); a1 = fmaf(w3, f1.w, a1);
     }
-    float bb = g_b2[o];
+    float bb = p.g_b2[o];
     h2[(rg * 2 + 0) * 64 + o] = fmaxf(a0 + bb, 0.f);
     h2[(rg * 2 + 1) * 64 + o] = fmaxf(a1 + bb, 0.f);
   }
@@ -610,23 +604,23 @@
     float a = 0.f;
     #pragma unroll 4
     for (int k4 = 0; k4 < 16; k4++) {
-      float w0 = g_w3t[(k4 * 4 + 0) * 32 + o];
-      float w1 = g_w3t[(k4 * 4 + 1) * 32 + o];
-      float w2 = g_w3t[(k4 * 4 + 2) * 32 + o];
-      float w3 = g_w3t[(k4 * 4 + 3) * 32 + o];
+      float w0 = p.g3t[(k4 * 4 + 0) * 32 + o];
+      float w1 = p.g3t[(k4 * 4 + 1) * 32 + o];
+      float w2 = p.g3t[(k4 * 4 + 2) * 32 + o];
+      float w3 = p.g3t[(k4 * 4 + 3) * 32 + o];
       float4 f0 = *(const float4*)(fp + k4 * 4);
       a = fmaf(w0, f0.x, a); a = fmaf(w1, f0.y, a);
       a = fmaf(w2, f0.z, a); a = fmaf(w3, f0.w, a);
     }
-    h3[rg * 32 + o] = fmaxf(a + g_b3[o], 0.f);
+    h3[rg * 32 + o] = fmaxf(a + p.g_b3[o], 0.f);
   }
   __syncthreads();
   if (tid < 32) {
     int r = tid >> 2, o = tid & 3;
     const float* hh = h3 + r * 32;
-    float a = g_b4[o];
+    float a = p.g_b4[o];
     #pragma unroll
-    for (int k = 0; k < 32; k++) a = fmaf(g_w4t[k * 4 + o], hh[k], a);
+    for (int k = 0; k < 32; k++) a = fmaf(p.g4t[k * 4 + o], hh[k], a);
     lg[tid] = a;
   }
   __syncthreads();
@@ -638,75 +632,84 @@
     float e2 = __expf(l2 - m), e3 = __expf(l3 - m);
     float is = __builtin_amdgcn_rcpf(e0 + e1 + e2 + e3);
     float4 o4; o4.x = e0 * is; o4.y = e1 * is; o4.z = e2 * is; o4.w = e3 * is;
-    *(float4*)(out + (size_t)(b0 + tid) * 4) = o4;
+    *(float4*)(p.out + (size_t)(b0 + tid) * 4) = o4;
+  }
+}
+
+__global__ __launch_bounds__(256) void k_main(KP p) {
+  __shared__ __align__(16) char smem[SM_BYTES];
+  const int bid = blockIdx.x;
+  const int tid = threadIdx.x;
+  if (bid < 512) {
+    lstm_block(bid, tid, p, smem);
+  } else if (bid < 640) {
+    prep2_block(bid - 512, tid, p);
+  } else if (bid < 1664) {
+    stats_block(bid - 640, tid, p, smem);
+  } else {
+    head_block(bid - 1664, tid, p, smem);
   }
 }
 
 extern "C" void kernel_launch(void* const* d_in, const int* in_sizes, int n_in,
                               void* d_out, int out_size, void* d_ws, size_t ws_size,
                               hipStream_t stream) {
-  const int*   x     = (const int*)d_in[0];
-  const float* emb   = (const float*)d_in[1];
-  const float* wih_f = (const float*)d_in[2];
-  const float* whh_f = (const float*)d_in[3];
-  const float* bih_f = (const float*)d_in[4];
-  const float* bhh_f = (const float*)d_in[5];
-  const float* wih_r = (const float*)d_in[6];
-  const float* whh_r = (const float*)d_in[7];
-  const float* bih_r = (const float*)d_in[8];
-  const float* bhh_r = (const float*)d_in[9];
-  const float* e_w1 = (const float*)d_in[10]; const float* e_b1 = (const float*)d_in[11];
-  const float* e_w2 = (const float*)d_in[12]; const float* e_b2 = (const float*)d_in[13];
-  const float* l_w1 = (const float*)d_in[14]; const float* l_b1 = (const float*)d_in[15];
-  const float* l_w2 = (const float*)d_in[16]; const float* l_b2 = (const float*)d_in[17];
-  const float* c_w1 = (const float*)d_in[18]; const float* c_b1 = (const float*)d_in[19];
-  const float* c_w2 = (const float*)d_in[20]; const float* c_b2 = (const float*)d_in[21];
-  const float* p_w1 = (const float*)d_in[22]; const float* p_b1 = (const float*)d_in[23];
-  const float* p_w2 = (const float*)d_in[24]; const float* p_b2 = (const float*)d_in[25];
-  const float* x_w1 = (const float*)d_in[26]; const float* x_b1 = (const float*)d_in[27];
-  const float* x_w2 = (const float*)d_in[28]; const float* x_b2 = (const float*)d_in[29];
-  const float* fp_w = (const float*)d_in[30]; const float* fp_b = (const float*)d_in[31];
-  const float* attn_w = (const float*)d_in[32]; const float* attn_b = (const float*)d_in[33];
-  const float* out_w = (const float*)d_in[34]; const float* out_b = (const float*)d_in[35];
-  const float* g_w1 = (const float*)d_in[36]; const float* g_b1 = (const float*)d_in[37];
-  const float* g_w2 = (const float*)d_in[38]; const float* g_b2 = (const float*)d_in[39];
-  const float* g_w3 = (const float*)d_in[40]; const float* g_b3 = (const float*)d_in[41];
-  const float* g_w4 = (const float*)d_in[42]; const float* g_b4 = (const float*)d_in[43];
-
-  float* ws   = (float*)d_ws;
-  float* G_f  = ws;
-  float* G_r  = G_f  + 512 * 256;
-  float* hfw  = G_r  + 512 * 256;
-  float* hrw  = hfw  + BATCH * 64;
-  float* entw = hrw  + BATCH * 64;
-  float* vlnw = entw + BATCH;
-  float* patw = vlnw + BATCH;
-  float* cpxw = patw + BATCH * 6;
-  float* Aw   = cpxw + BATCH * 4;
-  float* avbw = Aw + 128 * ADJ;
-  float* Bpw  = avbw + 128;
-  float* vbw  = Bpw + ADJ * 180;
-  float* C1t  = vbw + ADJ;
-  float* c1b  = C1t + 180 * 128;
-  float* g2t  = c1b + 128;
-  float* g3t  = g2t + 128 * 64;
-  float* g4t  = g3t + 64 * 32;
-  float* cw1t = g4t + 32 * 4;
-  unsigned short* Wfrag = (unsigned short*)(cw1t + 512 * 32);
-
-  k_prep<<<dim3(465), dim3(256), 0, stream>>>(
-      emb, wih_f, bih_f, bhh_f, wih_r, bih_r, bhh_r, whh_f, whh_r,
-      g_w1, g_b1, out_w, out_b, attn_w, attn_b, fp_w, fp_b,
-      g_w2, g_w3, g_w4, c_w1,
-      G_f, G_r, Wfrag, Aw, avbw, Bpw, vbw, g2t, g3t, g4t, cw1t);
-  k_main<<<dim3(1664), dim3(256), 0, stream>>>(
-      x, G_f, G_r, Wfrag, Aw, avbw, Bpw, vbw, C1t, c1b,
-      hfw, hrw, entw, vlnw, patw, cpxw);
-  k_head<<<dim3(BATCH / 8), dim3(256), 0, stream>>>(
-      x, hfw, hrw, entw, vlnw, patw, cpxw,
-      e_w1, e_b1, e_w2, e_b2, l_w1, l_b1, l_w2, l_b2,
-      cw1t, c_b1, c_w2, c_b2, p_w1, p_b1, p_w2, p_b2,
-      x_w1, x_b1, x_w2, x_b2, C1t, c1b,
-      g2t, g_b2, g3t, g_b3, g4t, g_b4,
-      (float*)d_out);
-}
+  KP p;
+  p.x     = (const int*)d_in[0];
+  p.emb   = (const float*)d_in[1];
+  p.wih_f = (const float*)d_in[2];
+  p.whh_f = (const float*)d_in[3];
+  p.bif   = (const float*)d_in[4];
+  p.bhf   = (const float*)d_in[5];
+  p.wih_r = (const float*)d_in[6];
+  p.whh_r = (const float*)d_in[7];
+  p.bir   = (const float*)d_in[8];
+  p.bhr   = (const float*)d_in[9];
+  p.e_w1 = (const float*)d_in[10]; p.e_b1 = (const float*)d_in[11];
+  p.e_w2 = (const float*)d_in[12]; p.e_b2 = (const float*)d_in[13];
+  p.l_w1 = (const float*)d_in[14]; p.l_b1 = (const float*)d_in[15];
+  p.l_w2 = (const float*)d_in[16]; p.l_b2 = (const float*)d_in[17];
+  p.c_w1 = (const float*)d_in[18]; p.c_b1 = (const float*)d_in[19];
+  p.c_w2 = (const float*)d_in[20]; p.c_b2 = (const float*)d_in[21];
+  p.p_w1 = (const float*)d_in[22]; p.p_b1 = (const float*)d_in[23];
+  p.p_w2 = (const float*)d_in[24]; p.p_b2 = (const float*)d_in[25];
+  p.x_w1 = (const float*)d_in[26]; p.x_b1 = (const float*)d_in[27];
+  p.x_w2 = (const float*)d_in[28]; p.x_b2 = (const float*)d_in[29];
+  p.fp_w = (const float*)d_in[30]; p.fp_b = (const float*)d_in[31];
+  p.attn_w = (const float*)d_in[32]; p.attn_b = (const float*)d_in[33];
+  p.out_w = (const float*)d_in[34]; p.out_b = (const float*)d_in[35];
+  p.g_w1 = (const float*)d_in[36]; p.g_b1 = (const float*)d_in[37];
+  p.g_w2 = (const float*)d_in[38]; p.g_b2 = (const float*)d_in[39];
+  p.g_w3 = (const float*)d_in[40]; p.g_b3 = (const float*)d_in[41];
+  p.g_w4 = (const float*)d_in[42]; p.g_b4 = (const float*)d_in[43];
+
+  float* ws = (float*)d_ws;
+  p.G_f  = ws;
+  p.G_r  = p.G_f + 512 * 256;
+  p.hf   = p.G_r + 512 * 256;
+  p.hr   = p.hf + BATCH * 64;
+  p.ent  = p.hr + BATCH * 64;
+  p.vlen = p.ent + BATCH;
+  p.pat  = p.vlen + BATCH;
+  p.cpx  = p.pat + BATCH * 6;
+  p.A    = p.cpx + BATCH * 4;
+  p.avb  = p.A + 128 * ADJ;
+  p.Bp   = p.avb + 128;
+  p.vb   = p.Bp + ADJ * 180;
+  p.C1t  = p.vb + ADJ;
+  p.c1b  = p.C1t + 180 * 128;
+  p.g2t  = p.c1b + 128;
+  p.g3t  = p.g2t + 128 * 64;
+  p.g4t  = p.g3t + 64 * 32;
+  p.cw1t = p.g4t + 32 * 4;
+  p.Wfrag = (unsigned short*)(p.cw1t + 512 * 32);
+  int* flags = (int*)(p.Wfrag + 32768);
+  p.lflag = flags;
+  p.sflag = flags + 512;
+  p.p2ctr = flags + 1536;
+  p.out  = (float*)d_out;
+
+  hipMemsetAsync((void*)flags, 0, 1540 * sizeof(int), stream);
+  k_prep<<<dim3(465), dim3(256), 0, stream>>>(p);
+  k_main<<<dim3(2176), dim3(256), 0, stream>>>(p);
+}
```

Result: slower. 396.3 us (+60.3%).
